# Performance work log

Hardware: AMD Instinct MI355X
Metric: run time of the kernel (lower is better)

## Reference

```python
import jax, jax.numpy as jnp
from jax import lax
import numpy as np

# dims (match init_kwargs config)
B, L, D = 32, 512, 32          # batch, seq_len, input_dim
H = 256                         # hidden_dim
E = 8                           # num_experts
PLEN, O = 96, 32                # pred_len, output_dim
LAT = 256                       # flow latent_dim
PD, NPROT = 64, 16              # prototype_dim, num_prototypes


def setup_inputs() -> dict:
    key = jax.random.key(0)
    ks = iter(jax.random.split(key, 40))
    def n(shape, scale=0.02):
        return (jax.random.normal(next(ks), shape, jnp.float32) * scale)
    inp = {
        'x': jax.random.normal(next(ks), (B, L, D), jnp.float32),
        # prototypes + projector (metric gating / diversity)
        'prototypes': n((NPROT, PD), 0.5),
        'Wp': n((PD, PD)), 'bp': jnp.zeros((PD,), jnp.float32),
        # expert_feature_extractor: Linear(7D->H), ReLU, Linear(H->PD), LayerNorm(PD)
        'Wf1': n((7 * D, H)), 'bf1': jnp.zeros((H,), jnp.float32),
        'Wf2': n((H, PD)), 'bf2': jnp.zeros((PD,), jnp.float32),
        'ln_g': jnp.ones((PD,), jnp.float32), 'ln_b': jnp.zeros((PD,), jnp.float32),
        # flow encoder (latent mapping of flattened window) + gating head
        'W1': n((L * D, H)), 'b1': jnp.zeros((H,), jnp.float32),
        'W2': n((H, LAT)), 'b2': jnp.zeros((LAT,), jnp.float32),
        'Wg': n((LAT, E)), 'bg': jnp.zeros((E,), jnp.float32),
        'log_temp': jnp.zeros((), jnp.float32),
        # stacked FFT+Mamba expert params (leading axis = expert)
        'Win': n((E, D, H)), 'b_in': jnp.zeros((E, H), jnp.float32),
        'Wfft': n((E, H, H)), 'b_fft': jnp.zeros((E, H), jnp.float32),
        'a_logit': n((E, H), 1.0),
        'Whead': n((E, H, PLEN * O)), 'b_head': jnp.zeros((E, PLEN * O), jnp.float32),
    }
    return inp


def _expert_features(x, Wf1, bf1, Wf2, bf2, ln_g, ln_b):
    # faithful to compute_expert_features: 7 per-channel stats -> MLP -> LayerNorm
    Lf = jnp.float32(x.shape[1])
    x_mean = x.mean(axis=1)
    x_std = x.std(axis=1, ddof=1)             # torch unbiased std
    x_min = x.min(axis=1)
    x_max = x.max(axis=1)
    x_diff_mean = jnp.diff(x, axis=1).mean(axis=1)
    x_trend = (x[:, -1, :] - x[:, 0, :]) / Lf
    x_fft_mag = jnp.abs(jnp.fft.fft(x, axis=1)).mean(axis=1)
    cf = jnp.concatenate([x_mean, x_std, x_min, x_max, x_diff_mean, x_trend, x_fft_mag], axis=1)
    h = jax.nn.relu(cf @ Wf1 + bf1)
    ef = h @ Wf2 + bf2
    mu = ef.mean(axis=-1, keepdims=True)
    var = ef.var(axis=-1, keepdims=True)
    return (ef - mu) / jnp.sqrt(var + 1e-5) * ln_g + ln_b


def reference(x, prototypes, Wp, bp, Wf1, bf1, Wf2, bf2, ln_g, ln_b,
              W1, b1, W2, b2, Wg, bg, log_temp,
              Win, b_in, Wfft, b_fft, a_logit, Whead, b_head):
    b, l, d = x.shape
    # --- metric-based gating ---
    ef = _expert_features(x, Wf1, bf1, Wf2, bf2, ln_g, ln_b)           # [B,PD]
    latent = jax.nn.relu(x.reshape(b, -1) @ W1 + b1) @ W2 + b2          # flow latent [B,LAT]
    lg = latent @ Wg + bg                                               # [B,E]
    proj = ef @ Wp + bp                                                 # prototype_projector
    d2 = ((proj[:, None, :] - prototypes[None, :, :]) ** 2).sum(-1)     # [B,NPROT]
    d2_per_expert = d2.reshape(b, E, NPROT // E).min(axis=-1)           # min dist to each expert's prototypes
    temp = jnp.clip(jnp.exp(log_temp), 0.1, 10.0)
    w = jax.nn.softmax((lg - d2_per_expert) / temp, axis=-1)            # [B,E]

    # --- FFT + Mamba-style experts (vmapped over stacked expert params) ---
    def expert(Win_e, b_in_e, Wfft_e, b_fft_e, a_logit_e, Whead_e, b_head_e):
        h = jnp.einsum('bld,dh->blh', x, Win_e) + b_in_e                # [B,L,H]
        f = jnp.einsum('blh,hk->blk', jnp.abs(jnp.fft.fft(h, axis=1)), Wfft_e) + b_fft_e
        u = jax.nn.relu(h + f)
        a = jax.nn.sigmoid(a_logit_e)                                   # per-channel decay
        def step(s, ut):
            s = a * s + (1.0 - a) * ut
            return s, None
        s_last, _ = lax.scan(step, jnp.zeros((b, H), x.dtype), jnp.swapaxes(u, 0, 1))
        return (s_last @ Whead_e + b_head_e).reshape(b, PLEN, O)

    outs = jax.vmap(expert)(Win, b_in, Wfft, b_fft, a_logit, Whead, b_head)  # [E,B,PLEN,O]
    y = jnp.einsum('be,ebpo->bpo', w, outs)
    return y
```

## Files before the change

kernel.cpp:

```cpp
#include <hip/hip_runtime.h>
#include <hip/hip_bf16.h>


typedef __hip_bfloat16 bf16;
typedef unsigned short u16;
typedef __attribute__((ext_vector_type(8))) short s8v;
typedef __attribute__((ext_vector_type(4))) float f4v;

#define MFMA_BF16(a,b,c) __builtin_amdgcn_mfma_f32_16x16x32_bf16(a,b,c,0,0,0)

#if __has_builtin(__builtin_amdgcn_sqrtf)
#define FSQRT(x) __builtin_amdgcn_sqrtf(x)
#else
#define FSQRT(x) sqrtf(x)
#endif
#if __has_builtin(__builtin_amdgcn_exp2f)
#define FEXP2(x) __builtin_amdgcn_exp2f(x)
#else
#define FEXP2(x) exp2f(x)
#endif
#if __has_builtin(__builtin_amdgcn_logf)
#define FLOG2(x) __builtin_amdgcn_logf(x)
#else
#define FLOG2(x) log2f(x)
#endif

#define GWF1 0
#define GW2  57344
#define GWF2 122880
#define GWP  139264
#define GPROT 143360
#define GWG  144384

__device__ __forceinline__ float bf2f(u16 u){
  union{ unsigned u32; float f; } w; w.u32 = ((unsigned)u) << 16; return w.f;
}
__device__ __forceinline__ u16 f2bf(float f){
  bf16 h = __float2bfloat16(f);
  union{ bf16 b; u16 u; } w; w.b = h; return w.u;
}
__device__ __forceinline__ u16 f2bf_fast(float f){
  union{ float f; unsigned u; } v; v.f = f;
  unsigned r = v.u + 0x7FFFu + ((v.u >> 16) & 1u);
  return (u16)(r >> 16);
}
__device__ __forceinline__ float ldg_(const void* p, long long i, bool bf){
  float r;
  if(bf) r = bf2f(((const u16*)p)[i]);
  else   r = ((const float*)p)[i];
  return r;
}
__device__ __forceinline__ bool bfflag(const void* ln_g){
  return ((const u16*)ln_g)[0] == 0x3F80;
}

__global__ void kx_cvt(const void* __restrict__ ln_g, const void* __restrict__ x,
                       u16* __restrict__ xbf){
  const bool bf = bfflag(ln_g);
  int i = (blockIdx.x*256 + threadIdx.x)*4;
  if(bf){
    ushort4 v = *(const ushort4*)((const u16*)x + i);
    *(ushort4*)(xbf+i) = v;
  } else {
    float4 f = *(const float4*)((const float*)x + i);
    ushort4 v; v.x=f2bf(f.x); v.y=f2bf(f.y); v.z=f2bf(f.z); v.w=f2bf(f.w);
    *(ushort4*)(xbf+i) = v;
  }
}

__global__ __launch_bounds__(256) void kt_all(const void* __restrict__ ln_g,
    const void* __restrict__ Win, const void* __restrict__ Wfft,
    const void* __restrict__ W1, const void* __restrict__ Whead,
    const void* __restrict__ Wf1, const void* __restrict__ W2,
    const void* __restrict__ Wf2, const void* __restrict__ Wp,
    const void* __restrict__ prot, const void* __restrict__ Wg,
    u16* __restrict__ WinTg, u16* __restrict__ WfftTg,
    u16* __restrict__ W1Tg, u16* __restrict__ WheadTg,
    u16* __restrict__ gw){
  const bool bf = bfflag(ln_g);
  __shared__ u16 tile[64][72];
  int bx = blockIdx.x, t = threadIdx.x;
  if(bx < 256){
    int i = bx*256 + t;
    int e = i >> 13, r = i & 8191;
    int c = r >> 5, d = r & 31;
    WinTg[i] = f2bf(ldg_(Win, (long long)e*8192 + d*256 + c, bf));
    return;
  }
  if(bx < 384){
    int idx = bx - 256;
    int e = idx >> 4, tl = idx & 15, kb = tl >> 2, cb = tl & 3;
    if(bf){
      for(int q=0;q<16;q++){
        int G = q*256 + t; int ki = G >> 6, ci = G & 63;
        tile[ci][ki] = ((const u16*)Wfft)[(long long)e*65536 + (long long)(kb*64+ki)*256 + cb*64+ci];
      }
    } else {
      for(int q=0;q<16;q++){
        int G = q*256 + t; int ki = G >> 6, ci = G & 63;
        tile[ci][ki] = f2bf(((const float*)Wfft)[(long long)e*65536 + (long long)(kb*64+ki)*256 + cb*64+ci]);
      }
    }
    __syncthreads();
    for(int q=0;q<16;q++){
      int G = q*256 + t; int ci = G >> 6, ki = G & 63;
      WfftTg[(long long)e*65536 + (long long)(cb*64+ci)*256 + kb*64+ki] = tile[ci][ki];
    }
    return;
  }
  if(bx < 1408){
    int idx = bx - 384;
    int kb = idx & 255, nb = idx >> 8;
    if(bf){
      for(int q=0;q<16;q++){
        int G = q*256 + t; int ki = G >> 6, ni = G & 63;
        tile[ni][ki] = ((const u16*)W1)[(long long)(kb*64+ki)*256 + nb*64+ni];
      }
    } else {
      for(int q=0;q<16;q++){
        int G = q*256 + t; int ki = G >> 6, ni = G & 63;
        tile[ni][ki] = f2bf(((const float*)W1)[(long long)(kb*64+ki)*256 + nb*64+ni]);
      }
    }
    __syncthreads();
    for(int q=0;q<16;q++){
      int G = q*256 + t; int ni = G >> 6, ki = G & 63;
      W1Tg[(long long)(nb*64+ni)*16384 + kb*64+ki] = tile[ni][ki];
    }
    return;
  }
  if(bx < 2944){
    int idx = bx - 1408;
    int e = idx / 192, rem = idx % 192;
    int kb = rem / 48, nb = rem % 48;
    if(bf){
      for(int q=0;q<16;q++){
        int G = q*256 + t; int ki = G >> 6, ni = G & 63;
        tile[ni][ki] = ((const u16*)Whead)[(long long)e*786432 + (long long)(kb*64+ki)*3072 + nb*64+ni];
      }
    } else {
      for(int q=0;q<16;q++){
        int G = q*256 + t; int ki = G >> 6, ni = G & 63;
        tile[ni][ki] = f2bf(((const float*)Whead)[(long long)e*786432 + (long long)(kb*64+ki)*3072 + nb*64+ni]);
      }
    }
    __syncthreads();
    for(int q=0;q<16;q++){
      int G = q*256 + t; int ni = G >> 6, ki = G & 63;
      WheadTg[(long long)e*786432 + (long long)(nb*64+ni)*256 + kb*64+ki] = tile[ni][ki];
    }
    return;
  }
  {
    int c = bx - 2944;
    const void* src; int dstbase, blkoff;
    if(c < 56)      { src=Wf1;  dstbase=GWF1;  blkoff=c; }
    else if(c <120) { src=W2;   dstbase=GW2;   blkoff=c-56; }
    else if(c <136) { src=Wf2;  dstbase=GWF2;  blkoff=c-120; }
    else if(c <140) { src=Wp;   dstbase=GWP;   blkoff=c-136; }
    else if(c <141) { src=prot; dstbase=GPROT; blkoff=0; }
    else            { src=Wg;   dstbase=GWG;   blkoff=c-141; }
    int i = blkoff*1024 + t*4;
    if(bf){
      ushort4 v = *(const ushort4*)((const u16*)src + i);
      *(ushort4*)(gw + dstbase + i) = v;
    } else {
      float4 f = *(const float4*)((const float*)src + i);
      ushort4 v; v.x=f2bf(f.x); v.y=f2bf(f.y); v.z=f2bf(f.z); v.w=f2bf(f.w);
      *(ushort4*)(gw + dstbase + i) = v;
    }
  }
}

__global__ __launch_bounds__(256) void k1_fft(const void* __restrict__ ln_g,
                                              const void* __restrict__ x,
                                              u16* __restrict__ Xr, u16* __restrict__ Xi,
                                              float* __restrict__ cf){
  const bool bf = bfflag(ln_g);
  __shared__ float xs[512], re[512], im[512];
  __shared__ float twr[256], twi[256];
  __shared__ float r0s[4], r1s[4], r2s[4], r3s[4];
  int b = blockIdx.x >> 5, d = blockIdx.x & 31;
  int t = threadIdx.x;
  {
    float rev = -(float)t * (1.f/512.f);
#if __has_builtin(__builtin_amdgcn_cosf) && __has_builtin(__builtin_amdgcn_sinf)
    twr[t] = __builtin_amdgcn_cosf(rev);
    twi[t] = __builtin_amdgcn_sinf(rev);
#else
    float ang = rev * 6.283185307179586f;
    twr[t] = cosf(ang); twi[t] = sinf(ang);
#endif
  }
  for(int i=t;i<512;i+=256){
    float v = ldg_(x, (long long)(b*512+i)*32 + d, bf);
    xs[i] = v;
    re[__brev((unsigned)i) >> 23] = v;
    im[i] = 0.f;
  }
  __syncthreads();
  float s=0.f, s2=0.f, mn=3.0e38f, mx=-3.0e38f;
  for(int i=t;i<512;i+=256){ float v=xs[i]; s+=v; s2+=v*v; mn=fminf(mn,v); mx=fmaxf(mx,v); }
  #pragma unroll
  for(int o=32;o>0;o>>=1){
    s  += __shfl_down(s,o);  s2 += __shfl_down(s2,o);
    mn = fminf(mn,__shfl_down(mn,o)); mx = fmaxf(mx,__shfl_down(mx,o));
  }
  int wv = t>>6, ln = t&63;
  if(ln==0){ r0s[wv]=s; r1s[wv]=s2; r2s[wv]=mn; r3s[wv]=mx; }
  __syncthreads();
  if(t==0){
    float S =r0s[0]+r0s[1]+r0s[2]+r0s[3];
    float S2=r1s[0]+r1s[1]+r1s[2]+r1s[3];
    float MN=fminf(fminf(r2s[0],r2s[1]),fminf(r2s[2],r2s[3]));
    float MX=fmaxf(fmaxf(r3s[0],r3s[1]),fmaxf(r3s[2],r3s[3]));
    float mean = S*(1.f/512.f);
    float var  = (S2 - S*S*(1.f/512.f))*(1.f/511.f);
    float* c = cf + b*224;
    c[d]      = mean;
    c[32+d]   = sqrtf(fmaxf(var,0.f));
    c[64+d]   = MN;
    c[96+d]   = MX;
    float dv = xs[511]-xs[0];
    c[128+d]  = dv*(1.f/511.f);
    c[160+d]  = dv*(1.f/512.f);
  }
  for(int st=1; st<=9; ++st){
    __syncthreads();
    int m = 1<<st, half = m>>1;
    int grp = t >> (st-1);
    int k   = t & (half-1);
    int i1 = grp*m + k, i2 = i1 + half;
    int ti_ = k << (9-st);
    float cs = twr[ti_], sn = twi[ti_];
    float ar=re[i1], ai=im[i1], br=re[i2], bi=im[i2];
    float tr = cs*br - sn*bi;
    float ti = cs*bi + sn*br;
    re[i1]=ar+tr; im[i1]=ai+ti;
    re[i2]=ar-tr; im[i2]=ai-ti;
  }
  __syncthreads();
  float ms=0.f;
  for(int i=t;i<512;i+=256){
    float rr=re[i], ii=im[i];
    long long o = (long long)(b*512+i)*32 + d;
    Xr[o]=f2bf(rr); Xi[o]=f2bf(ii);
    ms += FSQRT(rr*rr+ii*ii);
  }
  #pragma unroll
  for(int o=32;o>0;o>>=1) ms += __shfl_down(ms,o);
  if(ln==0) r0s[wv]=ms;
  __syncthreads();
  if(t==0) cf[b*224 + 192 + d] = (r0s[0]+r0s[1]+r0s[2]+r0s[3])*(1.f/512.f);
}

__global__ __launch_bounds__(256) void k3a_mfma(const u16* __restrict__ xbf,
                                                const u16* __restrict__ W1Tg,
                                                float* __restrict__ psum){
  int kb = blockIdx.x;
  int t = threadIdx.x;
  int w = t >> 6, lane = t & 63, quad = lane >> 4, l15 = lane & 15;
  const f4v zf = (f4v){0.f,0.f,0.f,0.f};
  f4v acc[2][4];
  #pragma unroll
  for(int mt=0;mt<2;mt++)
    #pragma unroll
    for(int nt=0;nt<4;nt++) acc[mt][nt] = zf;
  #pragma unroll
  for(int ks=0;ks<8;ks++){
    long long k = kb*256 + ks*32 + quad*8;
    s8v aF[2], bF[4];
    #pragma unroll
    for(int mt=0;mt<2;mt++)
      aF[mt] = *(const s8v*)(xbf + (long long)(mt*16 + l15)*16384 + k);
    #pragma unroll
    for(int nt=0;nt<4;nt++)
      bF[nt] = *(const s8v*)(W1Tg + (long long)(w*64 + nt*16 + l15)*16384 + k);
    #pragma unroll
    for(int mt=0;mt<2;mt++)
      #pragma unroll
      for(int nt=0;nt<4;nt++)
        acc[mt][nt] = MFMA_BF16(aF[mt], bF[nt], acc[mt][nt]);
  }
  float* po = psum + (long long)kb*8192;
  #pragma unroll
  for(int mt=0;mt<2;mt++)
    #pragma unroll
    for(int nt=0;nt<4;nt++)
      #pragma unroll
      for(int r=0;r<4;r++)
        po[(mt*16 + quad*4 + r)*256 + w*64 + nt*16 + l15] = acc[mt][nt][r];
}

__global__ __launch_bounds__(256) void kgate_a(
    const float* __restrict__ cf, const float* __restrict__ psum,
    const u16* __restrict__ gw,
    const void* __restrict__ bf1, const void* __restrict__ b1,
    const void* __restrict__ ln_g,
    float* __restrict__ hsf, float* __restrict__ h1f){
  const bool bf = bfflag(ln_g);
  int bx = blockIdx.x, t = threadIdx.x;
  if(bx < 32){
    int b = bx;
    float s0=0.f, s1=0.f, s2=0.f, s3=0.f;
    #pragma unroll
    for(int kb=0;kb<64;kb+=4){
      s0 += psum[(long long)(kb+0)*8192 + b*256 + t];
      s1 += psum[(long long)(kb+1)*8192 + b*256 + t];
      s2 += psum[(long long)(kb+2)*8192 + b*256 + t];
      s3 += psum[(long long)(kb+3)*8192 + b*256 + t];
    }
    hsf[b*256+t] = fmaxf((s0+s1)+(s2+s3) + ldg_(b1,t,bf), 0.f);
  } else {
    int b = bx - 32;
    __shared__ float cfs[224];
    if(t < 224) cfs[t] = cf[(long long)b*224 + t];
    __syncthreads();
    float a1 = ldg_(bf1, t, bf);
    const u16* Wp_ = gw + GWF1 + t;
    #pragma unroll 16
    for(int k=0;k<224;k++) a1 += cfs[k]*bf2f(Wp_[k*256]);
    h1f[b*256+t] = fmaxf(a1, 0.f);
  }
}

__global__ __launch_bounds__(256) void kgate_b(
    const float* __restrict__ hsf, const float* __restrict__ h1f,
    const u16* __restrict__ gw,
    const void* __restrict__ bf2, const void* __restrict__ ln_g,
    const void* __restrict__ ln_b, const void* __restrict__ bp,
    const void* __restrict__ b2, const void* __restrict__ bg,
    const void* __restrict__ log_temp,
    float* __restrict__ wgt){
  const bool bf = bfflag(ln_g);
  int b = blockIdx.x, t = threadIdx.x;
  __shared__ float hsL[256], h1L[256], latL[256], efL[64], prL[64];
  __shared__ float red[4][64];
  __shared__ float d2part[16][16], d2s[16], lgpart[32][8];

  hsL[t] = hsf[b*256+t];
  h1L[t] = h1f[b*256+t];
  __syncthreads();
  {
    float a = ldg_(b2, t, bf);
    const u16* W2p = gw + GW2 + t;
    #pragma unroll 16
    for(int k=0;k<256;k++) a += hsL[k]*bf2f(W2p[k*256]);
    latL[t] = a;
  }
  {
    int p = t>>6, j = t&63;
    float acc = 0.f;
    const u16* Wf2p = gw + GWF2 + p*64*64 + j;
    #pragma unroll 16
    for(int i=0;i<64;i++) acc += h1L[p*64+i]*bf2f(Wf2p[i*64]);
    red[p][j] = acc;
  }
  __syncthreads();
  if(t < 64){
    float a2 = red[0][t]+red[1][t]+red[2][t]+red[3][t] + ldg_(bf2,t,bf);
    float sm=a2, sq=a2*a2;
    #pragma unroll
    for(int o=32;o>0;o>>=1){ sm += __shfl_xor(sm,o); sq += __shfl_xor(sq,o); }
    float mu  = sm*(1.f/64.f);
    float var = sq*(1.f/64.f) - mu*mu;
    efL[t] = (a2-mu)*rsqrtf(fmaxf(var,0.f)+1e-5f)*ldg_(ln_g,t,bf) + ldg_(ln_b,t,bf);
    float p_acc = ldg_(bp, t, bf);
    const u16* Wpp = gw + GWP + t;
    #pragma unroll 16
    for(int k=0;k<64;k++) p_acc += efL[k]*bf2f(Wpp[k*64]);
    prL[t] = p_acc;
  }
  {
    int part = t>>3, e = t&7;
    float gp = 0.f;
    const u16* Wgp = gw + GWG + e;
    #pragma unroll
    for(int i=0;i<8;i++){
      int k = part*8 + i;
      gp += latL[k]*bf2f(Wgp[k*8]);
    }
    lgpart[part][e] = gp;
  }
  __syncthreads();
  {
    int p = t>>4, q4 = t&15;
    float dd = 0.f;
    #pragma unroll
    for(int i=0;i<4;i++){
      int d = q4*4 + i;
      float df = prL[d] - bf2f(gw[GPROT + p*64 + d]);
      dd += df*df;
    }
    d2part[p][q4] = dd;
  }
  __syncthreads();
  if(t < 16){
    float s = 0.f;
    #pragma unroll
    for(int i=0;i<16;i++) s += d2part[t][i];
    d2s[t] = s;
  }
  __syncthreads();
  if(t < 8){
    float g = ldg_(bg, t, bf);
    #pragma unroll
    for(int p=0;p<32;p++) g += lgpart[p][t];
    float d2pe = fminf(d2s[2*t], d2s[2*t+1]);
    float temp = fminf(fmaxf(__expf(ldg_(log_temp,0,bf)), 0.1f), 10.f);
    float v = (g - d2pe) / temp;
    float m = v;
    m = fmaxf(m, __shfl_xor(m,1));
    m = fmaxf(m, __shfl_xor(m,2));
    m = fmaxf(m, __shfl_xor(m,4));
    float ex = __expf(v-m);
    float sum = ex;
    sum += __shfl_xor(sum,1);
    sum += __shfl_xor(sum,2);
    sum += __shfl_xor(sum,4);
    wgt[b*8+t] = ex/sum;
  }
}

__global__ __launch_bounds__(256) void k5a_mag(const void* __restrict__ ln_g,
    const u16* __restrict__ Xr, const u16* __restrict__ Xi,
    const u16* __restrict__ WinTg, const void* __restrict__ b_in,
    u16* __restrict__ hmagG){
  const bool bf = bfflag(ln_g);
  int bx = blockIdx.x;
  int e = bx >> 7, inner = bx & 127;
  int b = inner >> 2, half = (inner >> 1) & 1, kh = inner & 1;
  int row0 = b*512 + half*128;
  int t = threadIdx.x;
  int w = t >> 6, lane = t & 63, quad = lane >> 4, l15 = lane & 15;
  __shared__ float binS[256];
  binS[t] = ldg_(b_in, e*256+t, bf);
  s8v xrF[2], xiF[2];
  #pragma unroll
  for(int nt=0;nt<2;nt++){
    long long row = row0 + w*32 + nt*16 + l15;
    xrF[nt] = *(const s8v*)(Xr + row*32 + quad*8);
    xiF[nt] = *(const s8v*)(Xi + row*32 + quad*8);
  }
  __syncthreads();
  u16* Ho = hmagG + (long long)((e<<6)|(b<<1)|half)*32768;
  const f4v zf = (f4v){0.f,0.f,0.f,0.f};
  #pragma unroll
  for(int kcl=0;kcl<2;kcl++){
    int k0 = (kh*2+kcl)*64;
    #pragma unroll
    for(int ct=0;ct<4;ct++){
      s8v wfr = *(const s8v*)(WinTg + ((long long)e*256 + k0 + ct*16 + l15)*32 + quad*8);
      #pragma unroll
      for(int nt=0;nt<2;nt++){
        f4v hr = MFMA_BF16(wfr, xrF[nt], zf);
        f4v hi = MFMA_BF16(wfr, xiF[nt], zf);
        int rowg = row0 + w*32 + nt*16 + l15;
        bool bin0 = ((rowg & 511) == 0);
        ushort4 pk;
        int cb4 = k0 + ct*16 + quad*4;
        float h0 = hr[0] + (bin0 ? 512.f*binS[cb4+0] : 0.f);
        float h1 = hr[1] + (bin0 ? 512.f*binS[cb4+1] : 0.f);
        float h2 = hr[2] + (bin0 ? 512.f*binS[cb4+2] : 0.f);
        float h3 = hr[3] + (bin0 ? 512.f*binS[cb4+3] : 0.f);
        pk.x = f2bf_fast(FSQRT(h0*h0 + hi[0]*hi[0]));
        pk.y = f2bf_fast(FSQRT(h1*h1 + hi[1]*hi[1]));
        pk.z = f2bf_fast(FSQRT(h2*h2 + hi[2]*hi[2]));
        pk.w = f2bf_fast(FSQRT(h3*h3 + hi[3]*hi[3]));
        *(ushort4*)&Ho[(w*32 + nt*16 + l15)*256 + cb4] = pk;
      }
    }
  }
}

__global__ __launch_bounds__(256) void k5b_gemm(const void* __restrict__ ln_g,
    const u16* __restrict__ xbf, const u16* __restrict__ hmagG,
    const u16* __restrict__ WinTg, const u16* __restrict__ WfftTg,
    const void* __restrict__ b_in, const void* __restrict__ b_fft,
    const void* __restrict__ a_logit, float* __restrict__ sp){
  const bool bf = bfflag(ln_g);
  int bx = blockIdx.x;
  int e = bx >> 7, inner = bx & 127;
  int b = inner >> 2, half = (inner >> 1) & 1, cb = inner & 1;
  int row0 = b*512 + half*128;
  int col0 = cb*128;
  int t = threadIdx.x;
  int w = t >> 6, lane = t & 63, quad = lane >> 4, l15 = lane & 15;

  __shared__ __align__(16) u16 BsT[128][72];
  __shared__ float biasS[128], l2aS[128], aS[128];

  if(t < 128){
    int c = col0 + t;
    biasS[t] = ldg_(b_in, e*256+c, bf) + ldg_(b_fft, e*256+c, bf);
    float a = 1.f/(1.f+__expf(-ldg_(a_logit, e*256+c, bf)));
    a = fminf(fmaxf(a, 1e-12f), 0.99999988f);
    aS[t] = a;
    l2aS[t] = FLOG2(a);
  }
  const u16* Ab = hmagG + (long long)((e<<6)|(b<<1)|half)*32768;
  const f4v zf = (f4v){0.f,0.f,0.f,0.f};
  f4v acc[2][8];
  #pragma unroll
  for(int mt=0;mt<2;mt++)
    #pragma unroll
    for(int nt=0;nt<8;nt++) acc[mt][nt] = zf;

  for(int kc=0;kc<4;kc++){
    int k0 = kc*64;
    __syncthreads();
    #pragma unroll
    for(int q=0;q<4;q++){
      int G = q*256 + t;
      int c = G >> 3, k8 = (G & 7)*8;
      *(s8v*)&BsT[c][k8] = *(const s8v*)(WfftTg + ((long long)e*256 + col0 + c)*256 + k0 + k8);
    }
    __syncthreads();
    #pragma unroll
    for(int ks=0;ks<2;ks++){
      int kb = ks*32 + quad*8;
      s8v aF0 = *(const s8v*)(Ab + (w*32 + l15)*256 + k0 + kb);
      s8v aF1 = *(const s8v*)(Ab + (w*32 + 16 + l15)*256 + k0 + kb);
      #pragma unroll
      for(int nt=0;nt<8;nt++){
        s8v bF = *(const s8v*)&BsT[nt*16 + l15][kb];
        acc[0][nt] = MFMA_BF16(aF0, bF, acc[0][nt]);
        acc[1][nt] = MFMA_BF16(aF1, bF, acc[1][nt]);
      }
    }
  }
  s8v xF[2], xFm[2];
  #pragma unroll
  for(int mt=0;mt<2;mt++){
    long long rowO = (long long)row0 + w*32 + mt*16 + l15;
    xF[mt] = *(const s8v*)(xbf + rowO*32 + quad*8);
    int lin = half*128 + w*32 + mt*16 + l15;
    int lm  = (512 - lin) & 511;
    xFm[mt] = *(const s8v*)(xbf + ((long long)b*512 + lm)*32 + quad*8);
  }
  int l0base = half*128 + w*32 + quad*4;
  float mz = (l0base == 0) ? 0.f : 1.f;
  float part[8];
  #pragma unroll
  for(int nt=0;nt<8;nt++){
    s8v wfh = *(const s8v*)(WinTg + ((long long)e*256 + col0 + nt*16 + l15)*32 + quad*8);
    f4v hv0 = MFMA_BF16(xF[0],  wfh, zf);
    f4v hv1 = MFMA_BF16(xF[1],  wfh, zf);
    f4v hm0 = MFMA_BF16(xFm[0], wfh, zf);
    f4v hm1 = MFMA_BF16(xFm[1], wfh, zf);
    int cl = nt*16 + l15;
    float l2a = l2aS[cl], bias = biasS[cl], av = aS[cl];
    float inv_a = FEXP2(-l2a);
    float cO0 = FEXP2(l2a * (float)(511 - l0base));
    float cO1 = FEXP2(l2a * (float)(495 - l0base));
    float cM0 = FEXP2(l2a * (float)(l0base - 1));
    float cM1 = FEXP2(l2a * (float)(l0base + 15));
    float sum = 0.f;
    #pragma unroll
    for(int r=0;r<4;r++){
      float u0 = fmaxf(acc[0][nt][r] + hv0[r] + bias, 0.f);
      sum += u0 * cO0;
      float u1 = fmaxf(acc[1][nt][r] + hv1[r] + bias, 0.f);
      sum += u1 * cO1;
      float m0 = fmaxf(acc[0][nt][r] + hm0[r] + bias, 0.f);
      float w0 = m0 * cM0;
      if(r == 0) w0 *= mz;
      sum += w0;
      float m1 = fmaxf(acc[1][nt][r] + hm1[r] + bias, 0.f);
      sum += m1 * cM1;
      cO0 *= inv_a; cO1 *= inv_a; cM0 *= av; cM1 *= av;
    }
    part[nt] = sum;
  }
  __syncthreads();
  float (*redS)[132] = (float(*)[132])BsT;
  #pragma unroll
  for(int nt=0;nt<8;nt++)
    redS[w*4 + quad][nt*16 + l15] = part[nt];
  __syncthreads();
  if(t < 128){
    float tot = 0.f;
    #pragma unroll
    for(int i=0;i<16;i++) tot += redS[i][t];
    sp[e*16384 + (b*2 + half)*256 + col0 + t] = tot;
  }
}

__global__ __launch_bounds__(256) void k5c(const void* __restrict__ ln_g,
    const float* __restrict__ sp, const float* __restrict__ wgt,
    const void* __restrict__ a_logit, const void* __restrict__ b_in,
    const void* __restrict__ b_fft, const u16* __restrict__ xbf,
    const u16* __restrict__ Xr, const u16* __restrict__ Xi,
    const void* __restrict__ Win, const void* __restrict__ Wfft,
    u16* __restrict__ ssbf){
  const bool bf = bfflag(ln_g);
  int e = blockIdx.x >> 5, b = blockIdx.x & 31, j = threadIdx.x;
  __shared__ float hm[256];
  __shared__ float xr6[32], xi6[32], x6[32];
  if(j < 32){
    long long o = ((long long)(b*512 + 256))*32 + j;
    xr6[j] = bf2f(Xr[o]);
    xi6[j] = bf2f(Xi[o]);
    x6[j]  = bf2f(xbf[o]);
  }
  __syncthreads();
  float sr=0.f, si=0.f, hx=0.f;
  if(bf){
    const u16* Wn = (const u16*)Win + (long long)e*8192 + j;
    #pragma unroll 8
    for(int d=0; d<32; d++){
      float wv = bf2f(Wn[d*256]);
      sr += xr6[d]*wv; si += xi6[d]*wv; hx += x6[d]*wv;
    }
  } else {
    const float* Wn = (const float*)Win + (long long)e*8192 + j;
    #pragma unroll 8
    for(int d=0; d<32; d++){
      float wv = Wn[d*256];
      sr += xr6[d]*wv; si += xi6[d]*wv; hx += x6[d]*wv;
    }
  }
  hm[j] = FSQRT(sr*sr + si*si);
  __syncthreads();
  float f = 0.f;
  if(bf){
    const u16* Wf = (const u16*)Wfft + (long long)e*65536 + j;
    #pragma unroll 8
    for(int k=0;k<256;k++) f += hm[k]*bf2f(Wf[(long long)k*256]);
  } else {
    const float* Wf = (const float*)Wfft + (long long)e*65536 + j;
    #pragma unroll 8
    for(int k=0;k<256;k++) f += hm[k]*Wf[(long long)k*256];
  }
  float a = 1.f/(1.f+__expf(-ldg_(a_logit, e*256+j, bf)));
  a = fminf(fmaxf(a, 1e-12f), 0.99999988f);
  float l2a = FLOG2(a);
  float u = fmaxf(hx + f + ldg_(b_in,e*256+j,bf) + ldg_(b_fft,e*256+j,bf), 0.f);
  float contrib = u * FEXP2(l2a * 255.f);
  const float* spe = sp + e*16384 + b*2*256;
  float sum = spe[j] + spe[256+j] + contrib;
  ssbf[(e*32+b)*256 + j] = f2bf(wgt[b*8+e]*(1.f-a)*sum);
}

__global__ __launch_bounds__(256) void k6_mfma(
    const u16* __restrict__ ssbf, const u16* __restrict__ WheadTg,
    float* __restrict__ yaccE){
  int nb = blockIdx.x, e = blockIdx.y;
  int t = threadIdx.x;
  int w = t >> 6, lane = t & 63, quad = lane >> 4, l15 = lane & 15;
  const f4v zf = (f4v){0.f,0.f,0.f,0.f};
  f4v acc[2][2];
  #pragma unroll
  for(int mt=0;mt<2;mt++)
    #pragma unroll
    for(int nt=0;nt<2;nt++) acc[mt][nt] = zf;
  #pragma unroll
  for(int ks=0;ks<8;ks++){
    int k = ks*32 + quad*8;
    s8v aF[2], bF[2];
    #pragma unroll
    for(int mt=0;mt<2;mt++)
      aF[mt] = *(const s8v*)(ssbf + (long long)(e*32 + mt*16 + l15)*256 + k);
    #pragma unroll
    for(int nt=0;nt<2;nt++)
      bF[nt] = *(const s8v*)(WheadTg + ((long long)e*3072 + nb*128 + w*32 + nt*16 + l15)*256 + k);
    #pragma unroll
    for(int mt=0;mt<2;mt++)
      #pragma unroll
      for(int nt=0;nt<2;nt++)
        acc[mt][nt] = MFMA_BF16(aF[mt], bF[nt], acc[mt][nt]);
  }
  float* yo = yaccE + (long long)e*98304;
  #pragma unroll
  for(int mt=0;mt<2;mt++)
    #pragma unroll
    for(int nt=0;nt<2;nt++){
      int col = nb*128 + w*32 + nt*16 + l15;
      #pragma unroll
      for(int r=0;r<4;r++){
        int b = mt*16 + quad*4 + r;
        yo[b*3072 + col] = acc[mt][nt][r];
      }
    }
}

__global__ void k7_out(const void* __restrict__ ln_g,
                       const float* __restrict__ yaccE,
                       const float* __restrict__ wgt,
                       const void* __restrict__ b_head,
                       void* __restrict__ out){
  const bool bf = bfflag(ln_g);
  int i = blockIdx.x*256 + threadIdx.x;
  int b = i / 3072, col = i - b*3072;
  float v = 0.f;
  #pragma unroll
  for(int e=0;e<8;e++)
    v += yaccE[(long long)e*98304 + i] + wgt[b*8+e]*ldg_(b_head, (long long)e*3072+col, bf);
  if(bf) ((u16*)out)[i] = f2bf(v);
  else   ((float*)out)[i] = v;
}

extern "C" void kernel_launch(void* const* d_in, const int* in_sizes, int n_in,
                              void* d_out, int out_size, void* d_ws, size_t ws_size,
                              hipStream_t stream){
  const void* x       = d_in[0];
  const void* prot    = d_in[1];
  const void* Wp      = d_in[2];
  const void* bp      = d_in[3];
  const void* Wf1     = d_in[4];
  const void* bf1     = d_in[5];
  const void* Wf2     = d_in[6];
  const void* bf2     = d_in[7];
  const void* ln_g    = d_in[8];
  const void* ln_b    = d_in[9];
  const void* W1      = d_in[10];
  const void* b1      = d_in[11];
  const void* W2      = d_in[12];
  const void* b2      = d_in[13];
  const void* Wg      = d_in[14];
  const void* bg      = d_in[15];
  const void* log_temp= d_in[16];
  const void* Win     = d_in[17];
  const void* b_in    = d_in[18];
  const void* Wfft    = d_in[19];
  const void* b_fft   = d_in[20];
  const void* a_logit = d_in[21];
  const void* Whead   = d_in[22];
  const void* b_head  = d_in[23];

  float* ws      = (float*)d_ws;
  float* cf      = ws;
  float* wgt     = cf + 7168;
  float* sp      = wgt + 256;
  float* hsf     = sp + 131072;
  float* h1f     = hsf + 8192;
  float* yaccE   = sp + 262144;
  float* psum    = yaccE + 786432;
  u16*   Xr      = (u16*)(psum + 524288);
  u16*   Xi      = Xr + 524288;
  u16*   xbf     = Xi + 524288;
  u16*   WinTg   = xbf + 524288;
  u16*   WfftTg  = WinTg + 65536;
  u16*   W1Tg    = WfftTg + 524288;
  u16*   WheadTg = W1Tg + 4194304;
  u16*   ssbf    = WheadTg + 6291456;
  u16*   gw      = ssbf + 65536;
  u16*   hmagG   = gw + 146432;

  kx_cvt   <<<dim3(512),   dim3(256), 0, stream>>>(ln_g, x, xbf);
  kt_all   <<<dim3(3087),  dim3(256), 0, stream>>>(ln_g, Win, Wfft, W1, Whead,
                                                   Wf1, W2, Wf2, Wp, prot, Wg,
                                                   WinTg, WfftTg, W1Tg, WheadTg, gw);
  k1_fft   <<<dim3(1024),  dim3(256), 0, stream>>>(ln_g, x, Xr, Xi, cf);
  k3a_mfma <<<dim3(64),    dim3(256), 0, stream>>>(xbf, W1Tg, psum);
  kgate_a  <<<dim3(64),    dim3(256), 0, stream>>>(cf, psum, gw, bf1, b1, ln_g,
                                                   hsf, h1f);
  kgate_b  <<<dim3(32),    dim3(256), 0, stream>>>(hsf, h1f, gw, bf2, ln_g, ln_b,
                                                   bp, b2, bg, log_temp, wgt);
  k5a_mag  <<<dim3(1024),  dim3(256), 0, stream>>>(ln_g, Xr, Xi, WinTg, b_in, hmagG);
  k5b_gemm <<<dim3(1024),  dim3(256), 0, stream>>>(ln_g, xbf, hmagG, WinTg, WfftTg,
                                                   b_in, b_fft, a_logit, sp);
  k5c      <<<dim3(256),   dim3(256), 0, stream>>>(ln_g, sp, wgt, a_logit, b_in, b_fft,
                                                   xbf, Xr, Xi, Win, Wfft, ssbf);
  k6_mfma  <<<dim3(24,8),  dim3(256), 0, stream>>>(ssbf, WheadTg, yaccE);
  k7_out   <<<dim3(384),   dim3(256), 0, stream>>>(ln_g, yaccE, wgt, b_head, d_out);
}
```

Before: 243.1 us.

## Merge independent kernels into shared-grid launches to cut launch count

Independent stages are merged into combined launches that dispatch on block index: x conversion, weight transposes and the per-channel FFT share one launch, and the gate GEMM runs beside the expert magnitude stage, so the gate path and expert path no longer serialize. The gating weight is moved out of the expert state computation and applied in the final output kernel, removing the dependency of expert state on the gate result. This trades fewer launches and cross-stage overlap for larger shared-memory footprints and mixed workloads inside one grid.

```diff
diff --git a/kernel.cpp b/kernel.cpp
--- a/kernel.cpp
+++ b/kernel.cpp
@@ -54,592 +54,593 @@
   return ((const u16*)ln_g)[0] == 0x3F80;
 }
 
-__global__ void kx_cvt(const void* __restrict__ ln_g, const void* __restrict__ x,
-                       u16* __restrict__ xbf){
-  const bool bf = bfflag(ln_g);
-  int i = (blockIdx.x*256 + threadIdx.x)*4;
-  if(bf){
-    ushort4 v = *(const ushort4*)((const u16*)x + i);
-    *(ushort4*)(xbf+i) = v;
-  } else {
-    float4 f = *(const float4*)((const float*)x + i);
-    ushort4 v; v.x=f2bf(f.x); v.y=f2bf(f.y); v.z=f2bf(f.z); v.w=f2bf(f.w);
-    *(ushort4*)(xbf+i) = v;
-  }
-}
-
-__global__ __launch_bounds__(256) void kt_all(const void* __restrict__ ln_g,
+__global__ __launch_bounds__(256) void ks1(const void* __restrict__ ln_g,
+    const void* __restrict__ x,
     const void* __restrict__ Win, const void* __restrict__ Wfft,
     const void* __restrict__ W1, const void* __restrict__ Whead,
     const void* __restrict__ Wf1, const void* __restrict__ W2,
     const void* __restrict__ Wf2, const void* __restrict__ Wp,
     const void* __restrict__ prot, const void* __restrict__ Wg,
+    u16* __restrict__ xbf,
     u16* __restrict__ WinTg, u16* __restrict__ WfftTg,
     u16* __restrict__ W1Tg, u16* __restrict__ WheadTg,
-    u16* __restrict__ gw){
-  const bool bf = bfflag(ln_g);
-  __shared__ u16 tile[64][72];
-  int bx = blockIdx.x, t = threadIdx.x;
-  if(bx < 256){
-    int i = bx*256 + t;
-    int e = i >> 13, r = i & 8191;
-    int c = r >> 5, d = r & 31;
-    WinTg[i] = f2bf(ldg_(Win, (long long)e*8192 + d*256 + c, bf));
-    return;
-  }
-  if(bx < 384){
-    int idx = bx - 256;
-    int e = idx >> 4, tl = idx & 15, kb = tl >> 2, cb = tl & 3;
-    if(bf){
-      for(int q=0;q<16;q++){
-        int G = q*256 + t; int ki = G >> 6, ci = G & 63;
-        tile[ci][ki] = ((const u16*)Wfft)[(long long)e*65536 + (long long)(kb*64+ki)*256 + cb*64+ci];
-      }
-    } else {
-      for(int q=0;q<16;q++){
-        int G = q*256 + t; int ki = G >> 6, ci = G & 63;
-        tile[ci][ki] = f2bf(((const float*)Wfft)[(long long)e*65536 + (long long)(kb*64+ki)*256 + cb*64+ci]);
-      }
-    }
-    __syncthreads();
-    for(int q=0;q<16;q++){
-      int G = q*256 + t; int ci = G >> 6, ki = G & 63;
-      WfftTg[(long long)e*65536 + (long long)(cb*64+ci)*256 + kb*64+ki] = tile[ci][ki];
-    }
-    return;
-  }
-  if(bx < 1408){
-    int idx = bx - 384;
-    int kb = idx & 255, nb = idx >> 8;
-    if(bf){
-      for(int q=0;q<16;q++){
-        int G = q*256 + t; int ki = G >> 6, ni = G & 63;
-        tile[ni][ki] = ((const u16*)W1)[(long long)(kb*64+ki)*256 + nb*64+ni];
-      }
-    } else {
-      for(int q=0;q<16;q++){
-        int G = q*256 + t; int ki = G >> 6, ni = G & 63;
-        tile[ni][ki] = f2bf(((const float*)W1)[(long long)(kb*64+ki)*256 + nb*64+ni]);
-      }
-    }
-    __syncthreads();
-    for(int q=0;q<16;q++){
-      int G = q*256 + t; int ni = G >> 6, ki = G & 63;
-      W1Tg[(long long)(nb*64+ni)*16384 + kb*64+ki] = tile[ni][ki];
-    }
-    return;
-  }
-  if(bx < 2944){
-    int idx = bx - 1408;
-    int e = idx / 192, rem = idx % 192;
-    int kb = rem / 48, nb = rem % 48;
-    if(bf){
-      for(int q=0;q<16;q++){
-        int G = q*256 + t; int ki = G >> 6, ni = G & 63;
-        tile[ni][ki] = ((const u16*)Whead)[(long long)e*786432 + (long long)(kb*64+ki)*3072 + nb*64+ni];
-      }
-    } else {
-      for(int q=0;q<16;q++){
-        int G = q*256 + t; int ki = G >> 6, ni = G & 63;
-        tile[ni][ki] = f2bf(((const float*)Whead)[(long long)e*786432 + (long long)(kb*64+ki)*3072 + nb*64+ni]);
-      }
-    }
-    __syncthreads();
-    for(int q=0;q<16;q++){
-      int G = q*256 + t; int ni = G >> 6, ki = G & 63;
-      WheadTg[(long long)e*786432 + (long long)(nb*64+ni)*256 + kb*64+ki] = tile[ni][ki];
-    }
-    return;
-  }
-  {
-    int c = bx - 2944;
-    const void* src; int dstbase, blkoff;
-    if(c < 56)      { src=Wf1;  dstbase=GWF1;  blkoff=c; }
-    else if(c <120) { src=W2;   dstbase=GW2;   blkoff=c-56; }
-    else if(c <136) { src=Wf2;  dstbase=GWF2;  blkoff=c-120; }
-    else if(c <140) { src=Wp;   dstbase=GWP;   blkoff=c-136; }
-    else if(c <141) { src=prot; dstbase=GPROT; blkoff=0; }
-    else            { src=Wg;   dstbase=GWG;   blkoff=c-141; }
-    int i = blkoff*1024 + t*4;
-    if(bf){
-      ushort4 v = *(const ushort4*)((const u16*)src + i);
-      *(ushort4*)(gw + dstbase + i) = v;
-    } else {
-      float4 f = *(const float4*)((const float*)src + i);
-      ushort4 v; v.x=f2bf(f.x); v.y=f2bf(f.y); v.z=f2bf(f.z); v.w=f2bf(f.w);
-      *(ushort4*)(gw + dstbase + i) = v;
-    }
-  }
-}
-
-__global__ __launch_bounds__(256) void k1_fft(const void* __restrict__ ln_g,
-                                              const void* __restrict__ x,
-                                              u16* __restrict__ Xr, u16* __restrict__ Xi,
-                                              float* __restrict__ cf){
+    u16* __restrict__ gw,
+    u16* __restrict__ Xr, u16* __restrict__ Xi, float* __restrict__ cf){
   const bool bf = bfflag(ln_g);
   __shared__ float xs[512], re[512], im[512];
   __shared__ float twr[256], twi[256];
   __shared__ float r0s[4], r1s[4], r2s[4], r3s[4];
-  int b = blockIdx.x >> 5, d = blockIdx.x & 31;
-  int t = threadIdx.x;
+  __shared__ u16 tile[64][72];
+  int BX = blockIdx.x, t = threadIdx.x;
+
+  if(BX < 1024){
+    int b = BX >> 5, d = BX & 31;
+    {
+      float rev = -(float)t * (1.f/512.f);
+#if __has_builtin(__builtin_amdgcn_cosf) && __has_builtin(__builtin_amdgcn_sinf)
+      twr[t] = __builtin_amdgcn_cosf(rev);
+      twi[t] = __builtin_amdgcn_sinf(rev);
+#else
+      float ang = rev * 6.283185307179586f;
+      twr[t] = cosf(ang); twi[t] = sinf(ang);
+#endif
+    }
+    for(int i=t;i<512;i+=256){
+      float v = ldg_(x, (long long)(b*512+i)*32 + d, bf);
+      xs[i] = v;
+      re[__brev((unsigned)i) >> 23] = v;
+      im[i] = 0.f;
+    }
+    __syncthreads();
+    float s=0.f, s2=0.f, mn=3.0e38f, mx=-3.0e38f;
+    for(int i=t;i<512;i+=256){ float v=xs[i]; s+=v; s2+=v*v; mn=fminf(mn,v); mx=fmaxf(mx,v); }
+    #pragma unroll
+    for(int o=32;o>0;o>>=1){
+      s  += __shfl_down(s,o);  s2 += __shfl_down(s2,o);
+      mn = fminf(mn,__shfl_down(mn,o)); mx = fmaxf(mx,__shfl_down(mx,o));
+    }
+    int wv = t>>6, ln = t&63;
+    if(ln==0){ r0s[wv]=s; r1s[wv]=s2; r2s[wv]=mn; r3s[wv]=mx; }
+    __syncthreads();
+    if(t==0){
+      float S =r0s[0]+r0s[1]+r0s[2]+r0s[3];
+      float S2=r1s[0]+r1s[1]+r1s[2]+r1s[3];
+      float MN=fminf(fminf(r2s[0],r2s[1]),fminf(r2s[2],r2s[3]));
+      float MX=fmaxf(fmaxf(r3s[0],r3s[1]),fmaxf(r3s[2],r3s[3]));
+      float mean = S*(1.f/512.f);
+      float var  = (S2 - S*S*(1.f/512.f))*(1.f/511.f);
+      float* c = cf + b*224;
+      c[d]      = mean;
+      c[32+d]   = sqrtf(fmaxf(var,0.f));
+      c[64+d]   = MN;
+      c[96+d]   = MX;
+      float dv = xs[511]-xs[0];
+      c[128+d]  = dv*(1.f/511.f);
+      c[160+d]  = dv*(1.f/512.f);
+    }
+    for(int st=1; st<=9; ++st){
+      __syncthreads();
+      int m = 1<<st, half = m>>1;
+      int grp = t >> (st-1);
+      int k   = t & (half-1);
+      int i1 = grp*m + k, i2 = i1 + half;
+      int ti_ = k << (9-st);
+      float cs = twr[ti_], sn = twi[ti_];
+      float ar=re[i1], ai=im[i1], br=re[i2], bi=im[i2];
+      float tr = cs*br - sn*bi;
+      float ti = cs*bi + sn*br;
+      re[i1]=ar+tr; im[i1]=ai+ti;
+      re[i2]=ar-tr; im[i2]=ai-ti;
+    }
+    __syncthreads();
+    float ms=0.f;
+    for(int i=t;i<512;i+=256){
+      float rr=re[i], ii=im[i];
+      long long o = (long long)(b*512+i)*32 + d;
+      Xr[o]=f2bf(rr); Xi[o]=f2bf(ii);
+      ms += FSQRT(rr*rr+ii*ii);
+    }
+    #pragma unroll
+    for(int o=32;o>0;o>>=1) ms += __shfl_down(ms,o);
+    if(ln==0) r0s[wv]=ms;
+    __syncthreads();
+    if(t==0) cf[b*224 + 192 + d] = (r0s[0]+r0s[1]+r0s[2]+r0s[3])*(1.f/512.f);
+    return;
+  }
+  if(BX < 4111){
+    int bx = BX - 1024;
+    if(bx < 256){
+      int i = bx*256 + t;
+      int e = i >> 13, r = i & 8191;
+      int c = r >> 5, d = r & 31;
+      WinTg[i] = f2bf(ldg_(Win, (long long)e*8192 + d*256 + c, bf));
+      return;
+    }
+    if(bx < 384){
+      int idx = bx - 256;
+      int e = idx >> 4, tl = idx & 15, kb = tl >> 2, cb = tl & 3;
+      if(bf){
+        for(int q=0;q<16;q++){
+          int G = q*256 + t; int ki = G >> 6, ci = G & 63;
+          tile[ci][ki] = ((const u16*)Wfft)[(long long)e*65536 + (long long)(kb*64+ki)*256 + cb*64+ci];
+        }
+      } else {
+        for(int q=0;q<16;q++){
+          int G = q*256 + t; int ki = G >> 6, ci = G & 63;
+          tile[ci][ki] = f2bf(((const float*)Wfft)[(long long)e*65536 + (long long)(kb*64+ki)*256 + cb*64+ci]);
+        }
+      }
+      __syncthreads();
+      for(int q=0;q<16;q++){
+        int G = q*256 + t; int ci = G >> 6, ki = G & 63;
+        WfftTg[(long long)e*65536 + (long long)(cb*64+ci)*256 + kb*64+ki] = tile[ci][ki];
+      }
+      return;
+    }
+    if(bx < 1408){
+      int idx = bx - 384;
+      int kb = idx & 255, nb = idx >> 8;
+      if(bf){
+        for(int q=0;q<16;q++){
+          int G = q*256 + t; int ki = G >> 6, ni = G & 63;
+          tile[ni][ki] = ((const u16*)W1)[(long long)(kb*64+ki)*256 + nb*64+ni];
+        }
+      } else {
+        for(int q=0;q<16;q++){
+          int G = q*256 + t; int ki = G >> 6, ni = G & 63;
+          tile[ni][ki] = f2bf(((const float*)W1)[(long long)(kb*64+ki)*256 + nb*64+ni]);
+        }
+      }
+      __syncthreads();
+      for(int q=0;q<16;q++){
+        int G = q*256 + t; int ni = G >> 6, ki = G & 63;
+        W1Tg[(long long)(nb*64+ni)*16384 + kb*64+ki] = tile[ni][ki];
+      }
+      return;
+    }
+    if(bx < 2944){
+      int idx = bx - 1408;
+      int e = idx / 192, rem = idx % 192;
+      int kb = rem / 48, nb = rem % 48;
+      if(bf){
+        for(int q=0;q<16;q++){
+          int G = q*256 + t; int ki = G >> 6, ni = G & 63;
+          tile[ni][ki] = ((const u16*)Whead)[(long long)e*786432 + (long long)(kb*64+ki)*3072 + nb*64+ni];
+        }
+      } else {
+        for(int q=0;q<16;q++){
+          int G = q*256 + t; int ki = G >> 6, ni = G & 63;
+          tile[ni][ki] = f2bf(((const float*)Whead)[(long long)e*786432 + (long long)(kb*64+ki)*3072 + nb*64+ni]);
+        }
+      }
+      __syncthreads();
+      for(int q=0;q<16;q++){
+        int G = q*256 + t; int ni = G >> 6, ki = G & 63;
+        WheadTg[(long long)e*786432 + (long long)(nb*64+ni)*256 + kb*64+ki] = tile[ni][ki];
+      }
+      return;
+    }
+    {
+      int c = bx - 2944;
+      const void* src; int dstbase, blkoff;
+      if(c < 56)      { src=Wf1;  dstbase=GWF1;  blkoff=c; }
+      else if(c <120) { src=W2;   dstbase=GW2;   blkoff=c-56; }
+      else if(c <136) { src=Wf2;  dstbase=GWF2;  blkoff=c-120; }
+      else if(c <140) { src=Wp;   dstbase=GWP;   blkoff=c-136; }
+      else if(c <141) { src=prot; dstbase=GPROT; blkoff=0; }
+      else            { src=Wg;   dstbase=GWG;   blkoff=c-141; }
+      int i = blkoff*1024 + t*4;
+      if(bf){
+        ushort4 v = *(const ushort4*)((const u16*)src + i);
+        *(ushort4*)(gw + dstbase + i) = v;
+      } else {
+        float4 f = *(const float4*)((const float*)src + i);
+        ushort4 v; v.x=f2bf(f.x); v.y=f2bf(f.y); v.z=f2bf(f.z); v.w=f2bf(f.w);
+        *(ushort4*)(gw + dstbase + i) = v;
+      }
+    }
+    return;
+  }
   {
-    float rev = -(float)t * (1.f/512.f);
-#if __has_builtin(__builtin_amdgcn_cosf) && __has_builtin(__builtin_amdgcn_sinf)
-    twr[t] = __builtin_amdgcn_cosf(rev);
-    twi[t] = __builtin_amdgcn_sinf(rev);
-#else
-    float ang = rev * 6.283185307179586f;
-    twr[t] = cosf(ang); twi[t] = sinf(ang);
-#endif
-  }
-  for(int i=t;i<512;i+=256){
-    float v = ldg_(x, (long long)(b*512+i)*32 + d, bf);
-    xs[i] = v;
-    re[__brev((unsigned)i) >> 23] = v;
-    im[i] = 0.f;
-  }
-  __syncthreads();
-  float s=0.f, s2=0.f, mn=3.0e38f, mx=-3.0e38f;
-  for(int i=t;i<512;i+=256){ float v=xs[i]; s+=v; s2+=v*v; mn=fminf(mn,v); mx=fmaxf(mx,v); }
-  #pragma unroll
-  for(int o=32;o>0;o>>=1){
-    s  += __shfl_down(s,o);  s2 += __shfl_down(s2,o);
-    mn = fminf(mn,__shfl_down(mn,o)); mx = fmaxf(mx,__shfl_down(mx,o));
-  }
-  int wv = t>>6, ln = t&63;
-  if(ln==0){ r0s[wv]=s; r1s[wv]=s2; r2s[wv]=mn; r3s[wv]=mx; }
-  __syncthreads();
-  if(t==0){
-    float S =r0s[0]+r0s[1]+r0s[2]+r0s[3];
-    float S2=r1s[0]+r1s[1]+r1s[2]+r1s[3];
-    float MN=fminf(fminf(r2s[0],r2s[1]),fminf(r2s[2],r2s[3]));
-    float MX=fmaxf(fmaxf(r3s[0],r3s[1]),fmaxf(r3s[2],r3s[3]));
-    float mean = S*(1.f/512.f);
-    float var  = (S2 - S*S*(1.f/512.f))*(1.f/511.f);
-    float* c = cf + b*224;
-    c[d]      = mean;
-    c[32+d]   = sqrtf(fmaxf(var,0.f));
-    c[64+d]   = MN;
-    c[96+d]   = MX;
-    float dv = xs[511]-xs[0];
-    c[128+d]  = dv*(1.f/511.f);
-    c[160+d]  = dv*(1.f/512.f);
-  }
-  for(int st=1; st<=9; ++st){
-    __syncthreads();
-    int m = 1<<st, half = m>>1;
-    int grp = t >> (st-1);
-    int k   = t & (half-1);
-    int i1 = grp*m + k, i2 = i1 + half;
-    int ti_ = k << (9-st);
-    float cs = twr[ti_], sn = twi[ti_];
-    float ar=re[i1], ai=im[i1], br=re[i2], bi=im[i2];
-    float tr = cs*br - sn*bi;
-    float ti = cs*bi + sn*br;
-    re[i1]=ar+tr; im[i1]=ai+ti;
-    re[i2]=ar-tr; im[i2]=ai-ti;
-  }
-  __syncthreads();
-  float ms=0.f;
-  for(int i=t;i<512;i+=256){
-    float rr=re[i], ii=im[i];
-    long long o = (long long)(b*512+i)*32 + d;
-    Xr[o]=f2bf(rr); Xi[o]=f2bf(ii);
-    ms += FSQRT(rr*rr+ii*ii);
-  }
-  #pragma unroll
-  for(int o=32;o>0;o>>=1) ms += __shfl_down(ms,o);
-  if(ln==0) r0s[wv]=ms;
-  __syncthreads();
-  if(t==0) cf[b*224 + 192 + d] = (r0s[0]+r0s[1]+r0s[2]+r0s[3])*(1.f/512.f);
-}
-
-__global__ __launch_bounds__(256) void k3a_mfma(const u16* __restrict__ xbf,
-                                                const u16* __restrict__ W1Tg,
-                                                float* __restrict__ psum){
-  int kb = blockIdx.x;
-  int t = threadIdx.x;
+    int i = ((BX-4111)*256 + t)*4;
+    if(bf){
+      ushort4 v = *(const ushort4*)((const u16*)x + i);
+      *(ushort4*)(xbf+i) = v;
+    } else {
+      float4 f = *(const float4*)((const float*)x + i);
+      ushort4 v; v.x=f2bf(f.x); v.y=f2bf(f.y); v.z=f2bf(f.z); v.w=f2bf(f.w);
+      *(ushort4*)(xbf+i) = v;
+    }
+  }
+}
+
+__global__ __launch_bounds__(256) void ks2(const void* __restrict__ ln_g,
+    const u16* __restrict__ xbf, const u16* __restrict__ Xr, const u16* __restrict__ Xi,
+    const u16* __restrict__ WinTg, const u16* __restrict__ W1Tg,
+    const void* __restrict__ b_in,
+    float* __restrict__ psum, u16* __restrict__ hmagG){
+  const bool bf = bfflag(ln_g);
+  int BX = blockIdx.x, t = threadIdx.x;
   int w = t >> 6, lane = t & 63, quad = lane >> 4, l15 = lane & 15;
   const f4v zf = (f4v){0.f,0.f,0.f,0.f};
-  f4v acc[2][4];
-  #pragma unroll
-  for(int mt=0;mt<2;mt++)
-    #pragma unroll
-    for(int nt=0;nt<4;nt++) acc[mt][nt] = zf;
-  #pragma unroll
-  for(int ks=0;ks<8;ks++){
-    long long k = kb*256 + ks*32 + quad*8;
-    s8v aF[2], bF[4];
+  __shared__ float binS[256];
+
+  if(BX < 64){
+    int kb = BX;
+    f4v acc[2][4];
     #pragma unroll
     for(int mt=0;mt<2;mt++)
-      aF[mt] = *(const s8v*)(xbf + (long long)(mt*16 + l15)*16384 + k);
-    #pragma unroll
-    for(int nt=0;nt<4;nt++)
-      bF[nt] = *(const s8v*)(W1Tg + (long long)(w*64 + nt*16 + l15)*16384 + k);
+      #pragma unroll
+      for(int nt=0;nt<4;nt++) acc[mt][nt] = zf;
+    #pragma unroll
+    for(int ks=0;ks<8;ks++){
+      long long k = kb*256 + ks*32 + quad*8;
+      s8v aF[2], bF[4];
+      #pragma unroll
+      for(int mt=0;mt<2;mt++)
+        aF[mt] = *(const s8v*)(xbf + (long long)(mt*16 + l15)*16384 + k);
+      #pragma unroll
+      for(int nt=0;nt<4;nt++)
+        bF[nt] = *(const s8v*)(W1Tg + (long long)(w*64 + nt*16 + l15)*16384 + k);
+      #pragma unroll
+      for(int mt=0;mt<2;mt++)
+        #pragma unroll
+        for(int nt=0;nt<4;nt++)
+          acc[mt][nt] = MFMA_BF16(aF[mt], bF[nt], acc[mt][nt]);
+    }
+    float* po = psum + (long long)kb*8192;
     #pragma unroll
     for(int mt=0;mt<2;mt++)
       #pragma unroll
       for(int nt=0;nt<4;nt++)
-        acc[mt][nt] = MFMA_BF16(aF[mt], bF[nt], acc[mt][nt]);
-  }
-  float* po = psum + (long long)kb*8192;
-  #pragma unroll
-  for(int mt=0;mt<2;mt++)
-    #pragma unroll
-    for(int nt=0;nt<4;nt++)
-      #pragma unroll
-      for(int r=0;r<4;r++)
-        po[(mt*16 + quad*4 + r)*256 + w*64 + nt*16 + l15] = acc[mt][nt][r];
-}
-
-__global__ __launch_bounds__(256) void kgate_a(
+        #pragma unroll
+        for(int r=0;r<4;r++)
+          po[(mt*16 + quad*4 + r)*256 + w*64 + nt*16 + l15] = acc[mt][nt][r];
+    return;
+  }
+  {
+    int bx = BX - 64;
+    int e = bx >> 7, inner = bx & 127;
+    int b = inner >> 2, half = (inner >> 1) & 1, kh = inner & 1;
+    int row0 = b*512 + half*128;
+    binS[t] = ldg_(b_in, e*256+t, bf);
+    s8v xrF[2], xiF[2];
+    #pragma unroll
+    for(int nt=0;nt<2;nt++){
+      long long row = row0 + w*32 + nt*16 + l15;
+      xrF[nt] = *(const s8v*)(Xr + row*32 + quad*8);
+      xiF[nt] = *(const s8v*)(Xi + row*32 + quad*8);
+    }
+    __syncthreads();
+    u16* Ho = hmagG + (long long)((e<<6)|(b<<1)|half)*32768;
+    #pragma unroll
+    for(int kcl=0;kcl<2;kcl++){
+      int k0 = (kh*2+kcl)*64;
+      #pragma unroll
+      for(int ct=0;ct<4;ct++){
+        s8v wfr = *(const s8v*)(WinTg + ((long long)e*256 + k0 + ct*16 + l15)*32 + quad*8);
+        #pragma unroll
+        for(int nt=0;nt<2;nt++){
+          f4v hr = MFMA_BF16(wfr, xrF[nt], zf);
+          f4v hi = MFMA_BF16(wfr, xiF[nt], zf);
+          int rowg = row0 + w*32 + nt*16 + l15;
+          bool bin0 = ((rowg & 511) == 0);
+          ushort4 pk;
+          int cb4 = k0 + ct*16 + quad*4;
+          float h0 = hr[0] + (bin0 ? 512.f*binS[cb4+0] : 0.f);
+          float h1 = hr[1] + (bin0 ? 512.f*binS[cb4+1] : 0.f);
+          float h2 = hr[2] + (bin0 ? 512.f*binS[cb4+2] : 0.f);
+          float h3 = hr[3] + (bin0 ? 512.f*binS[cb4+3] : 0.f);
+          pk.x = f2bf_fast(FSQRT(h0*h0 + hi[0]*hi[0]));
+          pk.y = f2bf_fast(FSQRT(h1*h1 + hi[1]*hi[1]));
+          pk.z = f2bf_fast(FSQRT(h2*h2 + hi[2]*hi[2]));
+          pk.w = f2bf_fast(FSQRT(h3*h3 + hi[3]*hi[3]));
+          *(ushort4*)&Ho[(w*32 + nt*16 + l15)*256 + cb4] = pk;
+        }
+      }
+    }
+  }
+}
+
+__global__ __launch_bounds__(256) void ks3(const void* __restrict__ ln_g,
     const float* __restrict__ cf, const float* __restrict__ psum,
     const u16* __restrict__ gw,
     const void* __restrict__ bf1, const void* __restrict__ b1,
-    const void* __restrict__ ln_g,
-    float* __restrict__ hsf, float* __restrict__ h1f){
+    const u16* __restrict__ xbf, const u16* __restrict__ hmagG,
+    const u16* __restrict__ WinTg, const u16* __restrict__ WfftTg,
+    const void* __restrict__ b_in, const void* __restrict__ b_fft,
+    const void* __restrict__ a_logit,
+    float* __restrict__ hsf, float* __restrict__ h1f, float* __restrict__ sp){
   const bool bf = bfflag(ln_g);
-  int bx = blockIdx.x, t = threadIdx.x;
-  if(bx < 32){
-    int b = bx;
-    float s0=0.f, s1=0.f, s2=0.f, s3=0.f;
-    #pragma unroll
-    for(int kb=0;kb<64;kb+=4){
-      s0 += psum[(long long)(kb+0)*8192 + b*256 + t];
-      s1 += psum[(long long)(kb+1)*8192 + b*256 + t];
-      s2 += psum[(long long)(kb+2)*8192 + b*256 + t];
-      s3 += psum[(long long)(kb+3)*8192 + b*256 + t];
-    }
-    hsf[b*256+t] = fmaxf((s0+s1)+(s2+s3) + ldg_(b1,t,bf), 0.f);
-  } else {
-    int b = bx - 32;
-    __shared__ float cfs[224];
-    if(t < 224) cfs[t] = cf[(long long)b*224 + t];
-    __syncthreads();
-    float a1 = ldg_(bf1, t, bf);
-    const u16* Wp_ = gw + GWF1 + t;
-    #pragma unroll 16
-    for(int k=0;k<224;k++) a1 += cfs[k]*bf2f(Wp_[k*256]);
-    h1f[b*256+t] = fmaxf(a1, 0.f);
-  }
-}
-
-__global__ __launch_bounds__(256) void kgate_b(
+  int BX = blockIdx.x, t = threadIdx.x;
+  __shared__ __align__(16) u16 BsT[128][72];
+  __shared__ float biasS[128], l2aS[128], aS[128];
+  __shared__ float cfs[224];
+
+  if(BX < 64){
+    int bx = BX;
+    if(bx < 32){
+      int b = bx;
+      float s0=0.f, s1=0.f, s2=0.f, s3=0.f;
+      #pragma unroll
+      for(int kb=0;kb<64;kb+=4){
+        s0 += psum[(long long)(kb+0)*8192 + b*256 + t];
+        s1 += psum[(long long)(kb+1)*8192 + b*256 + t];
+        s2 += psum[(long long)(kb+2)*8192 + b*256 + t];
+        s3 += psum[(long long)(kb+3)*8192 + b*256 + t];
+      }
+      hsf[b*256+t] = fmaxf((s0+s1)+(s2+s3) + ldg_(b1,t,bf), 0.f);
+    } else {
+      int b = bx - 32;
+      if(t < 224) cfs[t] = cf[(long long)b*224 + t];
+      __syncthreads();
+      float a1 = ldg_(bf1, t, bf);
+      const u16* Wp_ = gw + GWF1 + t;
+      #pragma unroll 16
+      for(int k=0;k<224;k++) a1 += cfs[k]*bf2f(Wp_[k*256]);
+      h1f[b*256+t] = fmaxf(a1, 0.f);
+    }
+    return;
+  }
+  {
+    int bx = BX - 64;
+    int e = bx >> 7, inner = bx & 127;
+    int b = inner >> 2, half = (inner >> 1) & 1, cb = inner & 1;
+    int row0 = b*512 + half*128;
+    int col0 = cb*128;
+    int w = t >> 6, lane = t & 63, quad = lane >> 4, l15 = lane & 15;
+
+    if(t < 128){
+      int c = col0 + t;
+      biasS[t] = ldg_(b_in, e*256+c, bf) + ldg_(b_fft, e*256+c, bf);
+      float a = 1.f/(1.f+__expf(-ldg_(a_logit, e*256+c, bf)));
+      a = fminf(fmaxf(a, 1e-12f), 0.99999988f);
+      aS[t] = a;
+      l2aS[t] = FLOG2(a);
+    }
+    const u16* Ab = hmagG + (long long)((e<<6)|(b<<1)|half)*32768;
+    const f4v zf = (f4v){0.f,0.f,0.f,0.f};
+    f4v acc[2][8];
+    #pragma unroll
+    for(int mt=0;mt<2;mt++)
+      #pragma unroll
+      for(int nt=0;nt<8;nt++) acc[mt][nt] = zf;
+
+    for(int kc=0;kc<4;kc++){
+      int k0 = kc*64;
+      __syncthreads();
+      #pragma unroll
+      for(int q=0;q<4;q++){
+        int G = q*256 + t;
+        int c = G >> 3, k8 = (G & 7)*8;
+        *(s8v*)&BsT[c][k8] = *(const s8v*)(WfftTg + ((long long)e*256 + col0 + c)*256 + k0 + k8);
+      }
+      __syncthreads();
+      #pragma unroll
+      for(int ks=0;ks<2;ks++){
+        int kb = ks*32 + quad*8;
+        s8v aF0 = *(const s8v*)(Ab + (w*32 + l15)*256 + k0 + kb);
+        s8v aF1 = *(const s8v*)(Ab + (w*32 + 16 + l15)*256 + k0 + kb);
+        #pragma unroll
+        for(int nt=0;nt<8;nt++){
+          s8v bF = *(const s8v*)&BsT[nt*16 + l15][kb];
+          acc[0][nt] = MFMA_BF16(aF0, bF, acc[0][nt]);
+          acc[1][nt] = MFMA_BF16(aF1, bF, acc[1][nt]);
+        }
+      }
+    }
+    s8v xF[2], xFm[2];
+    #pragma unroll
+    for(int mt=0;mt<2;mt++){
+      long long rowO = (long long)row0 + w*32 + mt*16 + l15;
+      xF[mt] = *(const s8v*)(xbf + rowO*32 + quad*8);
+      int lin = half*128 + w*32 + mt*16 + l15;
+      int lm  = (512 - lin) & 511;
+      xFm[mt] = *(const s8v*)(xbf + ((long long)b*512 + lm)*32 + quad*8);
+    }
+    int l0base = half*128 + w*32 + quad*4;
+    float mz = (l0base == 0) ? 0.f : 1.f;
+    const f4v zf2 = (f4v){0.f,0.f,0.f,0.f};
+    float part[8];
+    #pragma unroll
+    for(int nt=0;nt<8;nt++){
+      s8v wfh = *(const s8v*)(WinTg + ((long long)e*256 + col0 + nt*16 + l15)*32 + quad*8);
+      f4v hv0 = MFMA_BF16(xF[0],  wfh, zf2);
+      f4v hv1 = MFMA_BF16(xF[1],  wfh, zf2);
+      f4v hm0 = MFMA_BF16(xFm[0], wfh, zf2);
+      f4v hm1 = MFMA_BF16(xFm[1], wfh, zf2);
+      int cl = nt*16 + l15;
+      float l2a = l2aS[cl], bias = biasS[cl], av = aS[cl];
+      float inv_a = FEXP2(-l2a);
+      float cO0 = FEXP2(l2a * (float)(511 - l0base));
+      float cO1 = FEXP2(l2a * (float)(495 - l0base));
+      float cM0 = FEXP2(l2a * (float)(l0base - 1));
+      float cM1 = FEXP2(l2a * (float)(l0base + 15));
+      float sum = 0.f;
+      #pragma unroll
+      for(int r=0;r<4;r++){
+        float u0 = fmaxf(acc[0][nt][r] + hv0[r] + bias, 0.f);
+        sum += u0 * cO0;
+        float u1 = fmaxf(acc[1][nt][r] + hv1[r] + bias, 0.f);
+        sum += u1 * cO1;
+        float m0 = fmaxf(acc[0][nt][r] + hm0[r] + bias, 0.f);
+        float w0 = m0 * cM0;
+        if(r == 0) w0 *= mz;
+        sum += w0;
+        float m1 = fmaxf(acc[1][nt][r] + hm1[r] + bias, 0.f);
+        sum += m1 * cM1;
+        cO0 *= inv_a; cO1 *= inv_a; cM0 *= av; cM1 *= av;
+      }
+      part[nt] = sum;
+    }
+    __syncthreads();
+    float (*redS)[132] = (float(*)[132])BsT;
+    #pragma unroll
+    for(int nt=0;nt<8;nt++)
+      redS[w*4 + quad][nt*16 + l15] = part[nt];
+    __syncthreads();
+    if(t < 128){
+      float tot = 0.f;
+      #pragma unroll
+      for(int i=0;i<16;i++) tot += redS[i][t];
+      sp[e*16384 + (b*2 + half)*256 + col0 + t] = tot;
+    }
+  }
+}
+
+__global__ __launch_bounds__(256) void ks4(const void* __restrict__ ln_g,
     const float* __restrict__ hsf, const float* __restrict__ h1f,
     const u16* __restrict__ gw,
-    const void* __restrict__ bf2, const void* __restrict__ ln_g,
-    const void* __restrict__ ln_b, const void* __restrict__ bp,
-    const void* __restrict__ b2, const void* __restrict__ bg,
-    const void* __restrict__ log_temp,
-    float* __restrict__ wgt){
+    const void* __restrict__ bf2, const void* __restrict__ ln_b,
+    const void* __restrict__ bp, const void* __restrict__ b2,
+    const void* __restrict__ bg, const void* __restrict__ log_temp,
+    const float* __restrict__ sp, const void* __restrict__ a_logit,
+    const void* __restrict__ b_in, const void* __restrict__ b_fft,
+    const u16* __restrict__ xbf, const u16* __restrict__ Xr,
+    const u16* __restrict__ Xi,
+    const void* __restrict__ Win, const void* __restrict__ Wfft,
+    float* __restrict__ wgt, u16* __restrict__ ssbf){
   const bool bf = bfflag(ln_g);
-  int b = blockIdx.x, t = threadIdx.x;
+  int BX = blockIdx.x, t = threadIdx.x;
   __shared__ float hsL[256], h1L[256], latL[256], efL[64], prL[64];
   __shared__ float red[4][64];
   __shared__ float d2part[16][16], d2s[16], lgpart[32][8];
-
-  hsL[t] = hsf[b*256+t];
-  h1L[t] = h1f[b*256+t];
-  __syncthreads();
-  {
-    float a = ldg_(b2, t, bf);
-    const u16* W2p = gw + GW2 + t;
-    #pragma unroll 16
-    for(int k=0;k<256;k++) a += hsL[k]*bf2f(W2p[k*256]);
-    latL[t] = a;
-  }
-  {
-    int p = t>>6, j = t&63;
-    float acc = 0.f;
-    const u16* Wf2p = gw + GWF2 + p*64*64 + j;
-    #pragma unroll 16
-    for(int i=0;i<64;i++) acc += h1L[p*64+i]*bf2f(Wf2p[i*64]);
-    red[p][j] = acc;
-  }
-  __syncthreads();
-  if(t < 64){
-    float a2 = red[0][t]+red[1][t]+red[2][t]+red[3][t] + ldg_(bf2,t,bf);
-    float sm=a2, sq=a2*a2;
-    #pragma unroll
-    for(int o=32;o>0;o>>=1){ sm += __shfl_xor(sm,o); sq += __shfl_xor(sq,o); }
-    float mu  = sm*(1.f/64.f);
-    float var = sq*(1.f/64.f) - mu*mu;
-    efL[t] = (a2-mu)*rsqrtf(fmaxf(var,0.f)+1e-5f)*ldg_(ln_g,t,bf) + ldg_(ln_b,t,bf);
-    float p_acc = ldg_(bp, t, bf);
-    const u16* Wpp = gw + GWP + t;
-    #pragma unroll 16
-    for(int k=0;k<64;k++) p_acc += efL[k]*bf2f(Wpp[k*64]);
-    prL[t] = p_acc;
-  }
-  {
-    int part = t>>3, e = t&7;
-    float gp = 0.f;
-    const u16* Wgp = gw + GWG + e;
-    #pragma unroll
-    for(int i=0;i<8;i++){
-      int k = part*8 + i;
-      gp += latL[k]*bf2f(Wgp[k*8]);
-    }
-    lgpart[part][e] = gp;
-  }
-  __syncthreads();
-  {
-    int p = t>>4, q4 = t&15;
-    float dd = 0.f;
-    #pragma unroll
-    for(int i=0;i<4;i++){
-      int d = q4*4 + i;
-      float df = prL[d] - bf2f(gw[GPROT + p*64 + d]);
-      dd += df*df;
-    }
-    d2part[p][q4] = dd;
-  }
-  __syncthreads();
-  if(t < 16){
-    float s = 0.f;
-    #pragma unroll
-    for(int i=0;i<16;i++) s += d2part[t][i];
-    d2s[t] = s;
-  }
-  __syncthreads();
-  if(t < 8){
-    float g = ldg_(bg, t, bf);
-    #pragma unroll
-    for(int p=0;p<32;p++) g += lgpart[p][t];
-    float d2pe = fminf(d2s[2*t], d2s[2*t+1]);
-    float temp = fminf(fmaxf(__expf(ldg_(log_temp,0,bf)), 0.1f), 10.f);
-    float v = (g - d2pe) / temp;
-    float m = v;
-    m = fmaxf(m, __shfl_xor(m,1));
-    m = fmaxf(m, __shfl_xor(m,2));
-    m = fmaxf(m, __shfl_xor(m,4));
-    float ex = __expf(v-m);
-    float sum = ex;
-    sum += __shfl_xor(sum,1);
-    sum += __shfl_xor(sum,2);
-    sum += __shfl_xor(sum,4);
-    wgt[b*8+t] = ex/sum;
-  }
-}
-
-__global__ __launch_bounds__(256) void k5a_mag(const void* __restrict__ ln_g,
-    const u16* __restrict__ Xr, const u16* __restrict__ Xi,
-    const u16* __restrict__ WinTg, const void* __restrict__ b_in,
-    u16* __restrict__ hmagG){
-  const bool bf = bfflag(ln_g);
-  int bx = blockIdx.x;
-  int e = bx >> 7, inner = bx & 127;
-  int b = inner >> 2, half = (inner >> 1) & 1, kh = inner & 1;
-  int row0 = b*512 + half*128;
-  int t = threadIdx.x;
-  int w = t >> 6, lane = t & 63, quad = lane >> 4, l15 = lane & 15;
-  __shared__ float binS[256];
-  binS[t] = ldg_(b_in, e*256+t, bf);
-  s8v xrF[2], xiF[2];
-  #pragma unroll
-  for(int nt=0;nt<2;nt++){
-    long long row = row0 + w*32 + nt*16 + l15;
-    xrF[nt] = *(const s8v*)(Xr + row*32 + quad*8);
-    xiF[nt] = *(const s8v*)(Xi + row*32 + quad*8);
-  }
-  __syncthreads();
-  u16* Ho = hmagG + (long long)((e<<6)|(b<<1)|half)*32768;
-  const f4v zf = (f4v){0.f,0.f,0.f,0.f};
-  #pragma unroll
-  for(int kcl=0;kcl<2;kcl++){
-    int k0 = (kh*2+kcl)*64;
-    #pragma unroll
-    for(int ct=0;ct<4;ct++){
-      s8v wfr = *(const s8v*)(WinTg + ((long long)e*256 + k0 + ct*16 + l15)*32 + quad*8);
-      #pragma unroll
-      for(int nt=0;nt<2;nt++){
-        f4v hr = MFMA_BF16(wfr, xrF[nt], zf);
-        f4v hi = MFMA_BF16(wfr, xiF[nt], zf);
-        int rowg = row0 + w*32 + nt*16 + l15;
-        bool bin0 = ((rowg & 511) == 0);
-        ushort4 pk;
-        int cb4 = k0 + ct*16 + quad*4;
-        float h0 = hr[0] + (bin0 ? 512.f*binS[cb4+0] : 0.f);
-        float h1 = hr[1] + (bin0 ? 512.f*binS[cb4+1] : 0.f);
-        float h2 = hr[2] + (bin0 ? 512.f*binS[cb4+2] : 0.f);
-        float h3 = hr[3] + (bin0 ? 512.f*binS[cb4+3] : 0.f);
-        pk.x = f2bf_fast(FSQRT(h0*h0 + hi[0]*hi[0]));
-        pk.y = f2bf_fast(FSQRT(h1*h1 + hi[1]*hi[1]));
-        pk.z = f2bf_fast(FSQRT(h2*h2 + hi[2]*hi[2]));
-        pk.w = f2bf_fast(FSQRT(h3*h3 + hi[3]*hi[3]));
-        *(ushort4*)&Ho[(w*32 + nt*16 + l15)*256 + cb4] = pk;
-      }
-    }
-  }
-}
-
-__global__ __launch_bounds__(256) void k5b_gemm(const void* __restrict__ ln_g,
-    const u16* __restrict__ xbf, const u16* __restrict__ hmagG,
-    const u16* __restrict__ WinTg, const u16* __restrict__ WfftTg,
-    const void* __restrict__ b_in, const void* __restrict__ b_fft,
-    const void* __restrict__ a_logit, float* __restrict__ sp){
-  const bool bf = bfflag(ln_g);
-  int bx = blockIdx.x;
-  int e = bx >> 7, inner = bx & 127;
-  int b = inner >> 2, half = (inner >> 1) & 1, cb = inner & 1;
-  int row0 = b*512 + half*128;
-  int col0 = cb*128;
-  int t = threadIdx.x;
-  int w = t >> 6, lane = t & 63, quad = lane >> 4, l15 = lane & 15;
-
-  __shared__ __align__(16) u16 BsT[128][72];
-  __shared__ float biasS[128], l2aS[128], aS[128];
-
-  if(t < 128){
-    int c = col0 + t;
-    biasS[t] = ldg_(b_in, e*256+c, bf) + ldg_(b_fft, e*256+c, bf);
-    float a = 1.f/(1.f+__expf(-ldg_(a_logit, e*256+c, bf)));
-    a = fminf(fmaxf(a, 1e-12f), 0.99999988f);
-    aS[t] = a;
-    l2aS[t] = FLOG2(a);
-  }
-  const u16* Ab = hmagG + (long long)((e<<6)|(b<<1)|half)*32768;
-  const f4v zf = (f4v){0.f,0.f,0.f,0.f};
-  f4v acc[2][8];
-  #pragma unroll
-  for(int mt=0;mt<2;mt++)
-    #pragma unroll
-    for(int nt=0;nt<8;nt++) acc[mt][nt] = zf;
-
-  for(int kc=0;kc<4;kc++){
-    int k0 = kc*64;
-    __syncthreads();
-    #pragma unroll
-    for(int q=0;q<4;q++){
-      int G = q*256 + t;
-      int c = G >> 3, k8 = (G & 7)*8;
-      *(s8v*)&BsT[c][k8] = *(const s8v*)(WfftTg + ((long long)e*256 + col0 + c)*256 + k0 + k8);
-    }
-    __syncthreads();
-    #pragma unroll
-    for(int ks=0;ks<2;ks++){
-      int kb = ks*32 + quad*8;
-      s8v aF0 = *(const s8v*)(Ab + (w*32 + l15)*256 + k0 + kb);
-      s8v aF1 = *(const s8v*)(Ab + (w*32 + 16 + l15)*256 + k0 + kb);
-      #pragma unroll
-      for(int nt=0;nt<8;nt++){
-        s8v bF = *(const s8v*)&BsT[nt*16 + l15][kb];
-        acc[0][nt] = MFMA_BF16(aF0, bF, acc[0][nt]);
-        acc[1][nt] = MFMA_BF16(aF1, bF, acc[1][nt]);
-      }
-    }
-  }
-  s8v xF[2], xFm[2];
-  #pragma unroll
-  for(int mt=0;mt<2;mt++){
-    long long rowO = (long long)row0 + w*32 + mt*16 + l15;
-    xF[mt] = *(const s8v*)(xbf + rowO*32 + quad*8);
-    int lin = half*128 + w*32 + mt*16 + l15;
-    int lm  = (512 - lin) & 511;
-    xFm[mt] = *(const s8v*)(xbf + ((long long)b*512 + lm)*32 + quad*8);
-  }
-  int l0base = half*128 + w*32 + quad*4;
-  float mz = (l0base == 0) ? 0.f : 1.f;
-  float part[8];
-  #pragma unroll
-  for(int nt=0;nt<8;nt++){
-    s8v wfh = *(const s8v*)(WinTg + ((long long)e*256 + col0 + nt*16 + l15)*32 + quad*8);
-    f4v hv0 = MFMA_BF16(xF[0],  wfh, zf);
-    f4v hv1 = MFMA_BF16(xF[1],  wfh, zf);
-    f4v hm0 = MFMA_BF16(xFm[0], wfh, zf);
-    f4v hm1 = MFMA_BF16(xFm[1], wfh, zf);
-    int cl = nt*16 + l15;
-    float l2a = l2aS[cl], bias = biasS[cl], av = aS[cl];
-    float inv_a = FEXP2(-l2a);
-    float cO0 = FEXP2(l2a * (float)(511 - l0base));
-    float cO1 = FEXP2(l2a * (float)(495 - l0base));
-    float cM0 = FEXP2(l2a * (float)(l0base - 1));
-    float cM1 = FEXP2(l2a * (float)(l0base + 15));
-    float sum = 0.f;
-    #pragma unroll
-    for(int r=0;r<4;r++){
-      float u0 = fmaxf(acc[0][nt][r] + hv0[r] + bias, 0.f);
-      sum += u0 * cO0;
-      float u1 = fmaxf(acc[1][nt][r] + hv1[r] + bias, 0.f);
-      sum += u1 * cO1;
-      float m0 = fmaxf(acc[0][nt][r] + hm0[r] + bias, 0.f);
-      float w0 = m0 * cM0;
-      if(r == 0) w0 *= mz;
-      sum += w0;
-      float m1 = fmaxf(acc[1][nt][r] + hm1[r] + bias, 0.f);
-      sum += m1 * cM1;
-      cO0 *= inv_a; cO1 *= inv_a; cM0 *= av; cM1 *= av;
-    }
-    part[nt] = sum;
-  }
-  __syncthreads();
-  float (*redS)[132] = (float(*)[132])BsT;
-  #pragma unroll
-  for(int nt=0;nt<8;nt++)
-    redS[w*4 + quad][nt*16 + l15] = part[nt];
-  __syncthreads();
-  if(t < 128){
-    float tot = 0.f;
-    #pragma unroll
-    for(int i=0;i<16;i++) tot += redS[i][t];
-    sp[e*16384 + (b*2 + half)*256 + col0 + t] = tot;
-  }
-}
-
-__global__ __launch_bounds__(256) void k5c(const void* __restrict__ ln_g,
-    const float* __restrict__ sp, const float* __restrict__ wgt,
-    const void* __restrict__ a_logit, const void* __restrict__ b_in,
-    const void* __restrict__ b_fft, const u16* __restrict__ xbf,
-    const u16* __restrict__ Xr, const u16* __restrict__ Xi,
-    const void* __restrict__ Win, const void* __restrict__ Wfft,
-    u16* __restrict__ ssbf){
-  const bool bf = bfflag(ln_g);
-  int e = blockIdx.x >> 5, b = blockIdx.x & 31, j = threadIdx.x;
   __shared__ float hm[256];
   __shared__ float xr6[32], xi6[32], x6[32];
-  if(j < 32){
-    long long o = ((long long)(b*512 + 256))*32 + j;
-    xr6[j] = bf2f(Xr[o]);
-    xi6[j] = bf2f(Xi[o]);
-    x6[j]  = bf2f(xbf[o]);
-  }
-  __syncthreads();
-  float sr=0.f, si=0.f, hx=0.f;
-  if(bf){
-    const u16* Wn = (const u16*)Win + (long long)e*8192 + j;
-    #pragma unroll 8
-    for(int d=0; d<32; d++){
-      float wv = bf2f(Wn[d*256]);
-      sr += xr6[d]*wv; si += xi6[d]*wv; hx += x6[d]*wv;
-    }
-  } else {
-    const float* Wn = (const float*)Win + (long long)e*8192 + j;
-    #pragma unroll 8
-    for(int d=0; d<32; d++){
-      float wv = Wn[d*256];
-      sr += xr6[d]*wv; si += xi6[d]*wv; hx += x6[d]*wv;
-    }
-  }
-  hm[j] = FSQRT(sr*sr + si*si);
-  __syncthreads();
-  float f = 0.f;
-  if(bf){
-    const u16* Wf = (const u16*)Wfft + (long long)e*65536 + j;
-    #pragma unroll 8
-    for(int k=0;k<256;k++) f += hm[k]*bf2f(Wf[(long long)k*256]);
-  } else {
-    const float* Wf = (const float*)Wfft + (long long)e*65536 + j;
-    #pragma unroll 8
-    for(int k=0;k<256;k++) f += hm[k]*Wf[(long long)k*256];
-  }
-  float a = 1.f/(1.f+__expf(-ldg_(a_logit, e*256+j, bf)));
-  a = fminf(fmaxf(a, 1e-12f), 0.99999988f);
-  float l2a = FLOG2(a);
-  float u = fmaxf(hx + f + ldg_(b_in,e*256+j,bf) + ldg_(b_fft,e*256+j,bf), 0.f);
-  float contrib = u * FEXP2(l2a * 255.f);
-  const float* spe = sp + e*16384 + b*2*256;
-  float sum = spe[j] + spe[256+j] + contrib;
-  ssbf[(e*32+b)*256 + j] = f2bf(wgt[b*8+e]*(1.f-a)*sum);
+
+  if(BX < 32){
+    int b = BX;
+    hsL[t] = hsf[b*256+t];
+    h1L[t] = h1f[b*256+t];
+    __syncthreads();
+    {
+      float a = ldg_(b2, t, bf);
+      const u16* W2p = gw + GW2 + t;
+      #pragma unroll 16
+      for(int k=0;k<256;k++) a += hsL[k]*bf2f(W2p[k*256]);
+      latL[t] = a;
+    }
+    {
+      int p = t>>6, j = t&63;
+      float acc = 0.f;
+      const u16* Wf2p = gw + GWF2 + p*64*64 + j;
+      #pragma unroll 16
+      for(int i=0;i<64;i++) acc += h1L[p*64+i]*bf2f(Wf2p[i*64]);
+      red[p][j] = acc;
+    }
+    __syncthreads();
+    if(t < 64){
+      float a2 = red[0][t]+red[1][t]+red[2][t]+red[3][t] + ldg_(bf2,t,bf);
+      float sm=a2, sq=a2*a2;
+      #pragma unroll
+      for(int o=32;o>0;o>>=1){ sm += __shfl_xor(sm,o); sq += __shfl_xor(sq,o); }
+      float mu  = sm*(1.f/64.f);
+      float var = sq*(1.f/64.f) - mu*mu;
+      efL[t] = (a2-mu)*rsqrtf(fmaxf(var,0.f)+1e-5f)*ldg_(ln_g,t,bf) + ldg_(ln_b,t,bf);
+      float p_acc = ldg_(bp, t, bf);
+      const u16* Wpp = gw + GWP + t;
+      #pragma unroll 16
+      for(int k=0;k<64;k++) p_acc += efL[k]*bf2f(Wpp[k*64]);
+      prL[t] = p_acc;
+    }
+    {
+      int part = t>>3, e = t&7;
+      float gp = 0.f;
+      const u16* Wgp = gw + GWG + e;
+      #pragma unroll
+      for(int i=0;i<8;i++){
+        int k = part*8 + i;
+        gp += latL[k]*bf2f(Wgp[k*8]);
+      }
+      lgpart[part][e] = gp;
+    }
+    __syncthreads();
+    {
+      int p = t>>4, q4 = t&15;
+      float dd = 0.f;
+      #pragma unroll
+      for(int i=0;i<4;i++){
+        int d = q4*4 + i;
+        float df = prL[d] - bf2f(gw[GPROT + p*64 + d]);
+        dd += df*df;
+      }
+      d2part[p][q4] = dd;
+    }
+    __syncthreads();
+    if(t < 16){
+      float s = 0.f;
+      #pragma unroll
+      for(int i=0;i<16;i++) s += d2part[t][i];
+      d2s[t] = s;
+    }
+    __syncthreads();
+    if(t < 8){
+      float g = ldg_(bg, t, bf);
+      #pragma unroll
+      for(int p=0;p<32;p++) g += lgpart[p][t];
+      float d2pe = fminf(d2s[2*t], d2s[2*t+1]);
+      float temp = fminf(fmaxf(__expf(ldg_(log_temp,0,bf)), 0.1f), 10.f);
+      float v = (g - d2pe) / temp;
+      float m = v;
+      m = fmaxf(m, __shfl_xor(m,1));
+      m = fmaxf(m, __shfl_xor(m,2));
+      m = fmaxf(m, __shfl_xor(m,4));
+      float ex = __expf(v-m);
+      float sum = ex;
+      sum += __shfl_xor(sum,1);
+      sum += __shfl_xor(sum,2);
+      sum += __shfl_xor(sum,4);
+      wgt[b*8+t] = ex/sum;
+    }
+    return;
+  }
+  {
+    int bx = BX - 32;
+    int e = bx >> 5, b = bx & 31, j = t;
+    if(j < 32){
+      long long o = ((long long)(b*512 + 256))*32 + j;
+      xr6[j] = bf2f(Xr[o]);
+      xi6[j] = bf2f(Xi[o]);
+      x6[j]  = bf2f(xbf[o]);
+    }
+    __syncthreads();
+    float sr=0.f, si=0.f, hx=0.f;
+    if(bf){
+      const u16* Wn = (const u16*)Win + (long long)e*8192 + j;
+      #pragma unroll 8
+      for(int d=0; d<32; d++){
+        float wv = bf2f(Wn[d*256]);
+        sr += xr6[d]*wv; si += xi6[d]*wv; hx += x6[d]*wv;
+      }
+    } else {
+      const float* Wn = (const float*)Win + (long long)e*8192 + j;
+      #pragma unroll 8
+      for(int d=0; d<32; d++){
+        float wv = Wn[d*256];
+        sr += xr6[d]*wv; si += xi6[d]*wv; hx += x6[d]*wv;
+      }
+    }
+    hm[j] = FSQRT(sr*sr + si*si);
+    __syncthreads();
+    float f = 0.f;
+    if(bf){
+      const u16* Wf = (const u16*)Wfft + (long long)e*65536 + j;
+      #pragma unroll 8
+      for(int k=0;k<256;k++) f += hm[k]*bf2f(Wf[(long long)k*256]);
+    } else {
+      const float* Wf = (const float*)Wfft + (long long)e*65536 + j;
+      #pragma unroll 8
+      for(int k=0;k<256;k++) f += hm[k]*Wf[(long long)k*256];
+    }
+    float a = 1.f/(1.f+__expf(-ldg_(a_logit, e*256+j, bf)));
+    a = fminf(fmaxf(a, 1e-12f), 0.99999988f);
+    float l2a = FLOG2(a);
+    float u = fmaxf(hx + f + ldg_(b_in,e*256+j,bf) + ldg_(b_fft,e*256+j,bf), 0.f);
+    float contrib = u * FEXP2(l2a * 255.f);
+    const float* spe = sp + e*16384 + b*2*256;
+    float sum = spe[j] + spe[256+j] + contrib;
+    ssbf[(e*32+b)*256 + j] = f2bf((1.f-a)*sum);
+  }
 }
 
 __global__ __launch_bounds__(256) void k6_mfma(
@@ -695,7 +696,7 @@
   float v = 0.f;
   #pragma unroll
   for(int e=0;e<8;e++)
-    v += yaccE[(long long)e*98304 + i] + wgt[b*8+e]*ldg_(b_head, (long long)e*3072+col, bf);
+    v += wgt[b*8+e]*(yaccE[(long long)e*98304 + i] + ldg_(b_head, (long long)e*3072+col, bf));
   if(bf) ((u16*)out)[i] = f2bf(v);
   else   ((float*)out)[i] = v;
 }
@@ -747,21 +748,21 @@
   u16*   gw      = ssbf + 65536;
   u16*   hmagG   = gw + 146432;
 
-  kx_cvt   <<<dim3(512),   dim3(256), 0, stream>>>(ln_g, x, xbf);
-  kt_all   <<<dim3(3087),  dim3(256), 0, stream>>>(ln_g, Win, Wfft, W1, Whead,
-                                                   Wf1, W2, Wf2, Wp, prot, Wg,
-                                                   WinTg, WfftTg, W1Tg, WheadTg, gw);
-  k1_fft   <<<dim3(1024),  dim3(256), 0, stream>>>(ln_g, x, Xr, Xi, cf);
-  k3a_mfma <<<dim3(64),    dim3(256), 0, stream>>>(xbf, W1Tg, psum);
-  kgate_a  <<<dim3(64),    dim3(256), 0, stream>>>(cf, psum, gw, bf1, b1, ln_g,
-                                                   hsf, h1f);
-  kgate_b  <<<dim3(32),    dim3(256), 0, stream>>>(hsf, h1f, gw, bf2, ln_g, ln_b,
-                                                   bp, b2, bg, log_temp, wgt);
-  k5a_mag  <<<dim3(1024),  dim3(256), 0, stream>>>(ln_g, Xr, Xi, WinTg, b_in, hmagG);
-  k5b_gemm <<<dim3(1024),  dim3(256), 0, stream>>>(ln_g, xbf, hmagG, WinTg, WfftTg,
-                                                   b_in, b_fft, a_logit, sp);
-  k5c      <<<dim3(256),   dim3(256), 0, stream>>>(ln_g, sp, wgt, a_logit, b_in, b_fft,
-                                                   xbf, Xr, Xi, Win, Wfft, ssbf);
-  k6_mfma  <<<dim3(24,8),  dim3(256), 0, stream>>>(ssbf, WheadTg, yaccE);
-  k7_out   <<<dim3(384),   dim3(256), 0, stream>>>(ln_g, yaccE, wgt, b_head, d_out);
-}
+  ks1 <<<dim3(4623), dim3(256), 0, stream>>>(ln_g, x, Win, Wfft, W1, Whead,
+                                             Wf1, W2, Wf2, Wp, prot, Wg,
+                                             xbf, WinTg, WfftTg, W1Tg, WheadTg, gw,
+                                             Xr, Xi, cf);
+  ks2 <<<dim3(1088), dim3(256), 0, stream>>>(ln_g, xbf, Xr, Xi, WinTg, W1Tg,
+                                             b_in, psum, hmagG);
+  ks3 <<<dim3(1088), dim3(256), 0, stream>>>(ln_g, cf, psum, gw, bf1, b1,
+                                             xbf, hmagG, WinTg, WfftTg,
+                                             b_in, b_fft, a_logit,
+                                             hsf, h1f, sp);
+  ks4 <<<dim3(288),  dim3(256), 0, stream>>>(ln_g, hsf, h1f, gw, bf2, ln_b,
+                                             bp, b2, bg, log_temp,
+                                             sp, a_logit, b_in, b_fft,
+                                             xbf, Xr, Xi, Win, Wfft,
+                                             wgt, ssbf);
+  k6_mfma <<<dim3(24,8), dim3(256), 0, stream>>>(ssbf, WheadTg, yaccE);
+  k7_out  <<<dim3(384),  dim3(256), 0, stream>>>(ln_g, yaccE, wgt, b_head, d_out);
+}
```

Result: faster. 204.9 us (-15.7%).
